# Optimization experiments

Measured on AMD Instinct MI355X. Metric: run time of the kernel, lower is better.

## Reference

```python
import jax, jax.numpy as jnp
import numpy as np

DIM = 1024
HEADS = 16
HD = DIM // HEADS          # 64
HID = 4 * DIM              # 4096
TPF = 1374                 # tokens_per_frame
LR = 0.1
NS_ITERS = 5
TTT_STEPS = 2
B, S = 2, 4
SN = S * TPF               # 5496


def _newton_schulz(G, iters=NS_ITERS):
    """Muon Newton-Schulz orthogonalization (quintic iteration)."""
    a, b, c = 3.4445, -4.7750, 2.0315
    X = G / (jnp.linalg.norm(G) + 1e-7)
    transposed = G.shape[0] > G.shape[1]
    if transposed:
        X = X.T
    for _ in range(iters):
        A = X @ X.T                      # [m,m], m = min(rows, cols)
        X = a * X + (b * A + c * (A @ A)) @ X
    return X.T if transposed else X


def _muon_update(p, g):
    return p - LR * _newton_schulz(g)


def setup_inputs() -> dict:
    key = jax.random.key(0)
    ks = jax.random.split(key, 8)
    inp = {
        "x": jax.random.normal(ks[0], (B, SN, DIM), jnp.float32),
        "qkv_w": jax.random.normal(ks[1], (DIM, 3 * DIM), jnp.float32) * (DIM ** -0.5),
        "qkv_b": jnp.zeros((3 * DIM,), jnp.float32),
        "qn_scale": jnp.ones((HD,), jnp.float32),
        "qn_bias": jnp.zeros((HD,), jnp.float32),
        "kn_scale": jnp.ones((HD,), jnp.float32),
        "kn_bias": jnp.zeros((HD,), jnp.float32),
        # theta: lecun-normal scale (std = 1/sqrt(fan_in))
        "ttt_gate": jax.random.normal(ks[2], (DIM, HID), jnp.float32) * (DIM ** -0.5),
        "ttt_val": jax.random.normal(ks[3], (DIM, HID), jnp.float32) * (DIM ** -0.5),
        "ttt_proj": jax.random.normal(ks[4], (HID, DIM), jnp.float32) * (HID ** -0.5),
        "proj_w": jax.random.normal(ks[5], (DIM, DIM), jnp.float32) * (DIM ** -0.5),
        "proj_b": jnp.zeros((DIM,), jnp.float32),
    }
    return inp


def reference(x, qkv_w, qkv_b, qn_scale, qn_bias, kn_scale, kn_bias,
              ttt_gate, ttt_val, ttt_proj, proj_w, proj_b):
    Bx, SNx, _ = x.shape
    qkv = x @ qkv_w + qkv_b                       # [B, SN, 3*DIM]
    q, k, v = jnp.split(qkv, 3, axis=-1)
    q = q.reshape(Bx, SNx, HEADS, HD)
    k = k.reshape(Bx, SNx, HEADS, HD)
    # per-head L2 normalize then affine NormLayer (x*scale + bias)
    q = q / (jnp.linalg.norm(q, axis=-1, keepdims=True) + 1e-6) * qn_scale + qn_bias
    k = k / (jnp.linalg.norm(k, axis=-1, keepdims=True) + 1e-6) * kn_scale + kn_bias
    q_ttt = q.reshape(-1, DIM)                    # [B*SN, DIM]
    k_ttt = k.reshape(-1, DIM)
    # no short_conv param at init -> v_mixed is identity, so v_target == v
    v_ttt = v.reshape(-1, DIM)

    theta = {"gate": ttt_gate, "val": ttt_val, "proj": ttt_proj}

    def loss_fn(p):
        h = jax.nn.swish(k_ttt @ p["gate"]) * (k_ttt @ p["val"])   # [B*SN, HID]
        pred = h @ p["proj"]                                        # [B*SN, DIM]
        return jnp.mean((pred - v_ttt) ** 2)

    for _ in range(TTT_STEPS):
        grads = jax.grad(loss_fn)(theta)
        theta = {kk: _muon_update(theta[kk], grads[kk]) for kk in theta}

    h_q = jax.nn.swish(q_ttt @ theta["gate"]) * (q_ttt @ theta["val"])
    o = (h_q @ theta["proj"]) @ proj_w + proj_b
    return o.reshape(Bx, SNx, DIM)
```

## Files before the change

kernel.cpp:

```cpp
#include <hip/hip_runtime.h>
#include <stdint.h>

#define NTOK 10992
#define NTOKA 11264
#define PMi 4194304

typedef unsigned short u16;
typedef __attribute__((ext_vector_type(8))) __bf16 b8;
typedef __attribute__((ext_vector_type(4))) float f32x4;

__device__ __forceinline__ u16 f2b(float f) {
  union { float f; uint32_t u; } v; v.f = f;
  return (u16)((v.u + 0x7fffu + ((v.u >> 16) & 1u)) >> 16);
}
__device__ __forceinline__ float b2f(u16 b) {
  union { uint32_t u; float f; } v; v.u = ((uint32_t)b) << 16; return v.f;
}
__device__ __forceinline__ uint2 pk4(u16 a, u16 b, u16 c, u16 d) {
  uint2 r; r.x = (uint32_t)a | ((uint32_t)b << 16); r.y = (uint32_t)c | ((uint32_t)d << 16);
  return r;
}
__device__ __forceinline__ void gload16(const u16* g, u16* l) {
  __builtin_amdgcn_global_load_lds((const __attribute__((address_space(1))) void*)(const void*)g,
                                   (__attribute__((address_space(3))) void*)(void*)l, 16, 0, 0);
}

struct GA {
  const u16* A[3]; const u16* B[3];
  void* C[3]; u16* O1[3]; u16* OT[3];
  const void* E0[3]; const u16* E1[3];
  int lda[3], ldb[3];
  int M, N, K, ldc, ldo1, ldt, lde0, lde1;
  float p0, p1;
};

template <int EPI, int SPLIT>
__global__ __launch_bounds__(256, 2) void gemm_bt(GA g) {
  __shared__ u16 As[128 * 32];
  __shared__ u16 Bs[128 * 32];
  int bz = blockIdx.z, koff = 0, klen = g.K;
  if constexpr (SPLIT) { koff = (bz & 1) * (g.K >> 1); bz >>= 1; klen = g.K >> 1; }
  const u16* __restrict__ A = g.A[bz] + koff;
  const u16* __restrict__ B = g.B[bz] + koff;
  const int lda = g.lda[bz], ldb = g.ldb[bz];
  const int m0 = blockIdx.y * 128, n0 = blockIdx.x * 128;
  const int tid = threadIdx.x, w = tid >> 6, lane = tid & 63;
  const int wr = (w >> 1) * 64, wc = (w & 1) * 64;
  const int ln = lane & 15, lq = lane >> 4;

  f32x4 acc[4][4];
#pragma unroll
  for (int i = 0; i < 4; ++i)
#pragma unroll
    for (int j = 0; j < 4; ++j)
#pragma unroll
      for (int r = 0; r < 4; ++r) acc[i][j][r] = 0.f;

  const u16* Ag = A + (size_t)(m0 + 32 * w + (lane >> 2)) * lda + (lane & 3) * 8;
  const u16* Bg = B + (size_t)(n0 + 32 * w + (lane >> 2)) * ldb + (lane & 3) * 8;
  u16* AsW = &As[w * 1024];
  u16* BsW = &Bs[w * 1024];
  const int nkt = klen >> 5;

  for (int kt = 0; kt < nkt; ++kt) {
    __syncthreads();
    gload16(Ag, AsW);
    gload16(Ag + (size_t)16 * lda, AsW + 512);
    gload16(Bg, BsW);
    gload16(Bg + (size_t)16 * ldb, BsW + 512);
    Ag += 32; Bg += 32;
    __syncthreads();
    b8 af[4], bfr[4];
#pragma unroll
    for (int i = 0; i < 4; ++i) af[i] = *(const b8*)&As[(wr + i * 16 + ln) * 32 + lq * 8];
#pragma unroll
    for (int j = 0; j < 4; ++j) bfr[j] = *(const b8*)&Bs[(wc + j * 16 + ln) * 32 + lq * 8];
#pragma unroll
    for (int i = 0; i < 4; ++i)
#pragma unroll
      for (int j = 0; j < 4; ++j)
        acc[i][j] = __builtin_amdgcn_mfma_f32_16x16x32_bf16(af[i], bfr[j], acc[i][j], 0, 0, 0);
  }

  float* Cf = (float*)g.C[bz];
  u16* Cb = (u16*)g.C[bz];
  u16* O1 = g.O1[bz];
  const float* E0f = (const float*)g.E0[bz];
  const u16* E0b = (const u16*)g.E0[bz];
  const u16* E1b = g.E1[bz];

#pragma unroll
  for (int i = 0; i < 4; ++i) {
    const int mb = m0 + wr + i * 16 + lq * 4;
    if (mb >= g.M) continue;
#pragma unroll
    for (int j = 0; j < 4; ++j) {
      const int n = n0 + wc + j * 16 + ln;
      if (n >= g.N) continue;
      float vv[4];
#pragma unroll
      for (int r = 0; r < 4; ++r) vv[r] = acc[i][j][r];
      if constexpr (EPI == 0) {
#pragma unroll
        for (int r = 0; r < 4; ++r) Cb[(size_t)(mb + r) * g.ldc + n] = f2b(vv[r]);
      } else if constexpr (EPI == 1) {
        const float bias = E0f[n];
#pragma unroll
        for (int r = 0; r < 4; ++r) Cb[(size_t)(mb + r) * g.ldc + n] = f2b(vv[r] + bias);
      } else if constexpr (EPI == 5) {
        u16 cq[4], oq[4];
#pragma unroll
        for (int r = 0; r < 4; ++r) {
          const int m = mb + r;
          const float zg = b2f(E0b[(size_t)m * g.lde0 + n]);
          const float zv = b2f(E1b[(size_t)m * g.lde1 + n]);
          const float s = 1.f / (1.f + __expf(-zg));
          cq[r] = f2b(vv[r] * zv * s * (1.f + zg * (1.f - s)));
          oq[r] = f2b(vv[r] * zg * s);
        }
        *(uint2*)&Cb[(size_t)n * g.ldt + mb] = pk4(cq[0], cq[1], cq[2], cq[3]);
        *(uint2*)&O1[(size_t)n * g.ldt + mb] = pk4(oq[0], oq[1], oq[2], oq[3]);
      } else if constexpr (EPI == 6) {
        const float bias = E0f[n];
#pragma unroll
        for (int r = 0; r < 4; ++r) Cf[(size_t)(mb + r) * g.ldc + n] = vv[r] + bias;
      } else if constexpr (EPI == 8) {
#pragma unroll
        for (int r = 0; r < 4; ++r) atomicAdd(&Cf[(size_t)(mb + r) * g.ldc + n], vv[r]);
      } else if constexpr (EPI == 16) {
        uint2 old = *(const uint2*)&Cb[(size_t)n * 1024 + mb];
        u16 nq[4];
        nq[0] = f2b(b2f((u16)(old.x & 0xffff)) - 0.1f * vv[0]);
        nq[1] = f2b(b2f((u16)(old.x >> 16)) - 0.1f * vv[1]);
        nq[2] = f2b(b2f((u16)(old.y & 0xffff)) - 0.1f * vv[2]);
        nq[3] = f2b(b2f((u16)(old.y >> 16)) - 0.1f * vv[3]);
        *(uint2*)&Cb[(size_t)n * 1024 + mb] = pk4(nq[0], nq[1], nq[2], nq[3]);
        if (O1) {
#pragma unroll
          for (int r = 0; r < 4; ++r) O1[(size_t)(mb + r) * 4096 + n] = nq[r];
        }
      }
    }
  }
}

template <int EPI>
__global__ __launch_bounds__(256, 2) void gemm_gv(GA g) {
  __shared__ u16 As[128 * 32];
  __shared__ u16 Gs[128 * 32];
  __shared__ u16 Vs[128 * 32];
  const u16* __restrict__ A = g.A[0];
  const u16* __restrict__ G = g.B[0];
  const u16* __restrict__ V = g.B[1];
  const int lda = g.lda[0], ldb = g.ldb[0];
  const int m0 = blockIdx.y * 128, n0 = blockIdx.x * 128;
  const int tid = threadIdx.x, w = tid >> 6, lane = tid & 63;
  const int wr = (w >> 1) * 64, wc = (w & 1) * 64;
  const int ln = lane & 15, lq = lane >> 4;

  f32x4 ag[4][4], av[4][4];
#pragma unroll
  for (int i = 0; i < 4; ++i)
#pragma unroll
    for (int j = 0; j < 4; ++j)
#pragma unroll
      for (int r = 0; r < 4; ++r) { ag[i][j][r] = 0.f; av[i][j][r] = 0.f; }

  const u16* Agp = A + (size_t)(m0 + 32 * w + (lane >> 2)) * lda + (lane & 3) * 8;
  const u16* Ggp = G + (size_t)(n0 + 32 * w + (lane >> 2)) * ldb + (lane & 3) * 8;
  const u16* Vgp = V + (size_t)(n0 + 32 * w + (lane >> 2)) * ldb + (lane & 3) * 8;
  u16* AsW = &As[w * 1024];
  u16* GsW = &Gs[w * 1024];
  u16* VsW = &Vs[w * 1024];
  const int nkt = g.K >> 5;

  for (int kt = 0; kt < nkt; ++kt) {
    __syncthreads();
    gload16(Agp, AsW);
    gload16(Agp + (size_t)16 * lda, AsW + 512);
    gload16(Ggp, GsW);
    gload16(Ggp + (size_t)16 * ldb, GsW + 512);
    gload16(Vgp, VsW);
    gload16(Vgp + (size_t)16 * ldb, VsW + 512);
    Agp += 32; Ggp += 32; Vgp += 32;
    __syncthreads();
    b8 af[4], gf[4], vf[4];
#pragma unroll
    for (int i = 0; i < 4; ++i) af[i] = *(const b8*)&As[(wr + i * 16 + ln) * 32 + lq * 8];
#pragma unroll
    for (int j = 0; j < 4; ++j) gf[j] = *(const b8*)&Gs[(wc + j * 16 + ln) * 32 + lq * 8];
#pragma unroll
    for (int j = 0; j < 4; ++j) vf[j] = *(const b8*)&Vs[(wc + j * 16 + ln) * 32 + lq * 8];
#pragma unroll
    for (int i = 0; i < 4; ++i)
#pragma unroll
      for (int j = 0; j < 4; ++j) {
        ag[i][j] = __builtin_amdgcn_mfma_f32_16x16x32_bf16(af[i], gf[j], ag[i][j], 0, 0, 0);
        av[i][j] = __builtin_amdgcn_mfma_f32_16x16x32_bf16(af[i], vf[j], av[i][j], 0, 0, 0);
      }
  }

  u16* Zg = (u16*)g.C[0];
  u16* Zv = g.O1[0];
  u16* Hh = g.O1[1];
  u16* HT = g.OT[0];

#pragma unroll
  for (int i = 0; i < 4; ++i) {
    const int mb = m0 + wr + i * 16 + lq * 4;
    if (mb >= g.M) continue;
#pragma unroll
    for (int j = 0; j < 4; ++j) {
      const int n = n0 + wc + j * 16 + ln;
      if (n >= g.N) continue;
      u16 hq[4];
#pragma unroll
      for (int r = 0; r < 4; ++r) {
        const int m = mb + r;
        const float zg = ag[i][j][r];
        const float zv = av[i][j][r];
        const float s = 1.f / (1.f + __expf(-zg));
        const u16 hb = f2b(zg * s * zv);
        if constexpr (EPI == 0) {
          Zg[(size_t)m * g.ldc + n] = f2b(zg);
          Zv[(size_t)m * g.ldc + n] = f2b(zv);
          Hh[(size_t)m * g.ldc + n] = hb;
          hq[r] = hb;
        } else {
          Zg[(size_t)m * g.ldc + n] = hb;
        }
      }
      if constexpr (EPI == 0)
        *(uint2*)&HT[(size_t)n * g.ldt + mb] = pk4(hq[0], hq[1], hq[2], hq[3]);
    }
  }
}

__global__ __launch_bounds__(256, 2) void fused_gg(GA ggr, GA ggv, int ysplit) {
  __shared__ u16 As[128 * 32];
  __shared__ u16 Bs[128 * 32];
  __shared__ u16 Vs[128 * 32];
  const int tid = threadIdx.x, w = tid >> 6, lane = tid & 63;
  const int wr = (w >> 1) * 64, wc = (w & 1) * 64;
  const int ln = lane & 15, lq = lane >> 4;

  if ((int)blockIdx.y < ysplit) {
    const u16* __restrict__ A = ggv.A[0];
    const u16* __restrict__ G = ggv.B[0];
    const u16* __restrict__ V = ggv.B[1];
    const int lda = ggv.lda[0], ldb = ggv.ldb[0];
    const int m0 = blockIdx.y * 128, n0 = blockIdx.x * 128;
    f32x4 ag[4][4], av[4][4];
#pragma unroll
    for (int i = 0; i < 4; ++i)
#pragma unroll
      for (int j = 0; j < 4; ++j)
#pragma unroll
        for (int r = 0; r < 4; ++r) { ag[i][j][r] = 0.f; av[i][j][r] = 0.f; }
    const u16* Agp = A + (size_t)(m0 + 32 * w + (lane >> 2)) * lda + (lane & 3) * 8;
    const u16* Ggp = G + (size_t)(n0 + 32 * w + (lane >> 2)) * ldb + (lane & 3) * 8;
    const u16* Vgp = V + (size_t)(n0 + 32 * w + (lane >> 2)) * ldb + (lane & 3) * 8;
    u16* AsW = &As[w * 1024];
    u16* GsW = &Bs[w * 1024];
    u16* VsW = &Vs[w * 1024];
    const int nkt = ggv.K >> 5;
    for (int kt = 0; kt < nkt; ++kt) {
      __syncthreads();
      gload16(Agp, AsW);
      gload16(Agp + (size_t)16 * lda, AsW + 512);
      gload16(Ggp, GsW);
      gload16(Ggp + (size_t)16 * ldb, GsW + 512);
      gload16(Vgp, VsW);
      gload16(Vgp + (size_t)16 * ldb, VsW + 512);
      Agp += 32; Ggp += 32; Vgp += 32;
      __syncthreads();
      b8 af[4], gf[4], vf[4];
#pragma unroll
      for (int i = 0; i < 4; ++i) af[i] = *(const b8*)&As[(wr + i * 16 + ln) * 32 + lq * 8];
#pragma unroll
      for (int j = 0; j < 4; ++j) gf[j] = *(const b8*)&Bs[(wc + j * 16 + ln) * 32 + lq * 8];
#pragma unroll
      for (int j = 0; j < 4; ++j) vf[j] = *(const b8*)&Vs[(wc + j * 16 + ln) * 32 + lq * 8];
#pragma unroll
      for (int i = 0; i < 4; ++i)
#pragma unroll
        for (int j = 0; j < 4; ++j) {
          ag[i][j] = __builtin_amdgcn_mfma_f32_16x16x32_bf16(af[i], gf[j], ag[i][j], 0, 0, 0);
          av[i][j] = __builtin_amdgcn_mfma_f32_16x16x32_bf16(af[i], vf[j], av[i][j], 0, 0, 0);
        }
    }
    u16* Zg = (u16*)ggv.C[0];
    u16* Zv = ggv.O1[0];
    u16* Hh = ggv.O1[1];
    u16* HT = ggv.OT[0];
#pragma unroll
    for (int i = 0; i < 4; ++i) {
      const int mb = m0 + wr + i * 16 + lq * 4;
      if (mb >= ggv.M) continue;
#pragma unroll
      for (int j = 0; j < 4; ++j) {
        const int n = n0 + wc + j * 16 + ln;
        if (n >= ggv.N) continue;
        u16 hq[4];
#pragma unroll
        for (int r = 0; r < 4; ++r) {
          const int m = mb + r;
          const float zg = ag[i][j][r];
          const float zv = av[i][j][r];
          const float s = 1.f / (1.f + __expf(-zg));
          const u16 hb = f2b(zg * s * zv);
          Zg[(size_t)m * ggv.ldc + n] = f2b(zg);
          Zv[(size_t)m * ggv.ldc + n] = f2b(zv);
          Hh[(size_t)m * ggv.ldc + n] = hb;
          hq[r] = hb;
        }
        *(uint2*)&HT[(size_t)n * ggv.ldt + mb] = pk4(hq[0], hq[1], hq[2], hq[3]);
      }
    }
  } else {
    const int yy = (int)blockIdx.y - ysplit;
    int bz = yy >> 3;
    const int m0 = (yy & 7) * 128, n0 = blockIdx.x * 128;
    const int koff = (bz & 1) * (ggr.K >> 1); bz >>= 1;
    const int klen = ggr.K >> 1;
    const u16* __restrict__ A = ggr.A[bz] + koff;
    const u16* __restrict__ B = ggr.B[bz] + koff;
    const int lda = ggr.lda[bz], ldb = ggr.ldb[bz];
    f32x4 acc[4][4];
#pragma unroll
    for (int i = 0; i < 4; ++i)
#pragma unroll
      for (int j = 0; j < 4; ++j)
#pragma unroll
        for (int r = 0; r < 4; ++r) acc[i][j][r] = 0.f;
    const u16* Ag = A + (size_t)(m0 + 32 * w + (lane >> 2)) * lda + (lane & 3) * 8;
    const u16* Bg = B + (size_t)(n0 + 32 * w + (lane >> 2)) * ldb + (lane & 3) * 8;
    u16* AsW = &As[w * 1024];
    u16* BsW = &Bs[w * 1024];
    const int nkt = klen >> 5;
    for (int kt = 0; kt < nkt; ++kt) {
      __syncthreads();
      gload16(Ag, AsW);
      gload16(Ag + (size_t)16 * lda, AsW + 512);
      gload16(Bg, BsW);
      gload16(Bg + (size_t)16 * ldb, BsW + 512);
      Ag += 32; Bg += 32;
      __syncthreads();
      b8 af[4], bfr[4];
#pragma unroll
      for (int i = 0; i < 4; ++i) af[i] = *(const b8*)&As[(wr + i * 16 + ln) * 32 + lq * 8];
#pragma unroll
      for (int j = 0; j < 4; ++j) bfr[j] = *(const b8*)&Bs[(wc + j * 16 + ln) * 32 + lq * 8];
#pragma unroll
      for (int i = 0; i < 4; ++i)
#pragma unroll
        for (int j = 0; j < 4; ++j)
          acc[i][j] = __builtin_amdgcn_mfma_f32_16x16x32_bf16(af[i], bfr[j], acc[i][j], 0, 0, 0);
    }
    float* Cf = (float*)ggr.C[bz];
#pragma unroll
    for (int i = 0; i < 4; ++i) {
      const int mb = m0 + wr + i * 16 + lq * 4;
      if (mb >= ggr.M) continue;
#pragma unroll
      for (int j = 0; j < 4; ++j) {
        const int n = n0 + wc + j * 16 + ln;
        if (n >= ggr.N) continue;
#pragma unroll
        for (int r = 0; r < 4; ++r) atomicAdd(&Cf[(size_t)(mb + r) * ggr.ldc + n], acc[i][j][r]);
      }
    }
  }
}

__global__ __launch_bounds__(256, 2) void fused_mt(GA gt, GA gm) {
  __shared__ u16 As[64 * 32];
  __shared__ u16 Bs[64 * 32];
  const int bz = blockIdx.z;
  const int mp = ((int)blockIdx.y >= 16) ? 1 : 0;
  const GA& g = mp ? gm : gt;
  const int m0 = ((int)blockIdx.y - (mp ? 16 : 0)) * 64, n0 = blockIdx.x * 64;
  const u16* __restrict__ A = g.A[bz];
  const u16* __restrict__ B = g.B[bz];
  const int lda = g.lda[bz], ldb = g.ldb[bz];
  const int tid = threadIdx.x, w = tid >> 6, lane = tid & 63;
  const int wr = (w >> 1) * 32, wc = (w & 1) * 32;
  const int ln = lane & 15, lq = lane >> 4;

  f32x4 acc[2][2];
#pragma unroll
  for (int i = 0; i < 2; ++i)
#pragma unroll
    for (int j = 0; j < 2; ++j)
#pragma unroll
      for (int r = 0; r < 4; ++r) acc[i][j][r] = 0.f;

  const u16* Ag = A + (size_t)(m0 + 16 * w + (lane >> 2)) * lda + (lane & 3) * 8;
  const u16* Bg = B + (size_t)(n0 + 16 * w + (lane >> 2)) * ldb + (lane & 3) * 8;
  u16* AsW = &As[w * 512];
  u16* BsW = &Bs[w * 512];
  const int nkt = g.K >> 5;

  for (int kt = 0; kt < nkt; ++kt) {
    __syncthreads();
    gload16(Ag, AsW);
    gload16(Bg, BsW);
    Ag += 32; Bg += 32;
    __syncthreads();
    b8 af[2], bfr[2];
#pragma unroll
    for (int i = 0; i < 2; ++i) af[i] = *(const b8*)&As[(wr + i * 16 + ln) * 32 + lq * 8];
#pragma unroll
    for (int j = 0; j < 2; ++j) bfr[j] = *(const b8*)&Bs[(wc + j * 16 + ln) * 32 + lq * 8];
#pragma unroll
    for (int i = 0; i < 2; ++i)
#pragma unroll
      for (int j = 0; j < 2; ++j)
        acc[i][j] = __builtin_amdgcn_mfma_f32_16x16x32_bf16(af[i], bfr[j], acc[i][j], 0, 0, 0);
  }

  u16* Cb = (u16*)g.C[bz];
  const u16* E0b = (const u16*)g.E0[bz];
#pragma unroll
  for (int i = 0; i < 2; ++i) {
    const int mb = m0 + wr + i * 16 + lq * 4;
#pragma unroll
    for (int j = 0; j < 2; ++j) {
      const int n = n0 + wc + j * 16 + ln;
      if (mp) {
#pragma unroll
        for (int r = 0; r < 4; ++r) {
          const int m = mb + r;
          Cb[(size_t)m * g.ldc + n] = f2b(g.p0 * b2f(E0b[(size_t)m * g.lde0 + n]) + acc[i][j][r]);
        }
      } else {
#pragma unroll
        for (int r = 0; r < 4; ++r) Cb[(size_t)(mb + r) * g.ldc + n] = f2b(acc[i][j][r]);
      }
    }
  }
}

template <int EPI>
__global__ __launch_bounds__(256, 2) void gemm64(GA g) {
  if constexpr (EPI == 10 || EPI == 11 || EPI == 12) {
    if (blockIdx.x > blockIdx.y) return;
  }
  __shared__ u16 As[64 * 32];
  __shared__ u16 Bs[64 * 32];
  const int bz = blockIdx.z;
  const u16* __restrict__ A = g.A[bz];
  const u16* __restrict__ B = g.B[bz];
  const int lda = g.lda[bz], ldb = g.ldb[bz];
  const int m0 = blockIdx.y * 64, n0 = blockIdx.x * 64;
  const int tid = threadIdx.x, w = tid >> 6, lane = tid & 63;
  const int wr = (w >> 1) * 32, wc = (w & 1) * 32;
  const int ln = lane & 15, lq = lane >> 4;

  f32x4 acc[2][2];
#pragma unroll
  for (int i = 0; i < 2; ++i)
#pragma unroll
    for (int j = 0; j < 2; ++j)
#pragma unroll
      for (int r = 0; r < 4; ++r) acc[i][j][r] = 0.f;

  const u16* Ag = A + (size_t)(m0 + 16 * w + (lane >> 2)) * lda + (lane & 3) * 8;
  const u16* Bg = B + (size_t)(n0 + 16 * w + (lane >> 2)) * ldb + (lane & 3) * 8;
  u16* AsW = &As[w * 512];
  u16* BsW = &Bs[w * 512];
  const int nkt = g.K >> 5;

  for (int kt = 0; kt < nkt; ++kt) {
    __syncthreads();
    gload16(Ag, AsW);
    gload16(Bg, BsW);
    Ag += 32; Bg += 32;
    __syncthreads();
    b8 af[2], bfr[2];
#pragma unroll
    for (int i = 0; i < 2; ++i) af[i] = *(const b8*)&As[(wr + i * 16 + ln) * 32 + lq * 8];
#pragma unroll
    for (int j = 0; j < 2; ++j) bfr[j] = *(const b8*)&Bs[(wc + j * 16 + ln) * 32 + lq * 8];
#pragma unroll
    for (int i = 0; i < 2; ++i)
#pragma unroll
      for (int j = 0; j < 2; ++j)
        acc[i][j] = __builtin_amdgcn_mfma_f32_16x16x32_bf16(af[i], bfr[j], acc[i][j], 0, 0, 0);
  }

  u16* Cb = (u16*)g.C[bz];
  u16* OT = g.OT[bz];
  const u16* E0b = (const u16*)g.E0[bz];
  const u16* E1b = g.E1[bz];
  const bool offdiag = (blockIdx.x != blockIdx.y);

#pragma unroll
  for (int i = 0; i < 2; ++i) {
    const int mb = m0 + wr + i * 16 + lq * 4;
    if (mb >= g.M) continue;
#pragma unroll
    for (int j = 0; j < 2; ++j) {
      const int n = n0 + wc + j * 16 + ln;
      if (n >= g.N) continue;
      float vv[4];
#pragma unroll
      for (int r = 0; r < 4; ++r) vv[r] = acc[i][j][r];
      if constexpr (EPI == 0) {
#pragma unroll
        for (int r = 0; r < 4; ++r) Cb[(size_t)(mb + r) * g.ldc + n] = f2b(vv[r]);
      } else if constexpr (EPI == 2) {
        u16 cq[4];
#pragma unroll
        for (int r = 0; r < 4; ++r) {
          const int m = mb + r;
          const u16 ub = f2b((vv[r] - b2f(E0b[(size_t)m * g.lde0 + n])) * g.p0);
          Cb[(size_t)m * g.ldc + n] = ub;
          cq[r] = ub;
        }
        *(uint2*)&OT[(size_t)n * g.ldt + mb] = pk4(cq[0], cq[1], cq[2], cq[3]);
      } else if constexpr (EPI == 10) {
        u16 cq[4];
#pragma unroll
        for (int r = 0; r < 4; ++r) {
          cq[r] = f2b(vv[r]);
          Cb[(size_t)(mb + r) * g.ldc + n] = cq[r];
        }
        if (offdiag)
          *(uint2*)&Cb[(size_t)n * g.ldc + mb] = pk4(cq[0], cq[1], cq[2], cq[3]);
      } else if constexpr (EPI == 11) {
        u16 cq[4];
#pragma unroll
        for (int r = 0; r < 4; ++r) {
          cq[r] = f2b(g.p0 * b2f(E0b[(size_t)(mb + r) * g.lde0 + n]) + g.p1 * vv[r]);
          Cb[(size_t)(mb + r) * g.ldc + n] = cq[r];
        }
        if (offdiag)
          *(uint2*)&Cb[(size_t)n * g.ldc + mb] = pk4(cq[0], cq[1], cq[2], cq[3]);
      } else if constexpr (EPI == 12) {
        const uint2 t2u = *(const uint2*)&E1b[(size_t)n * g.lde1 + mb];
        const float t2v[4] = { b2f((u16)(t2u.x & 0xffff)), b2f((u16)(t2u.x >> 16)),
                               b2f((u16)(t2u.y & 0xffff)), b2f((u16)(t2u.y >> 16)) };
        u16 cq[4];
#pragma unroll
        for (int r = 0; r < 4; ++r) {
          const int m = mb + r;
          const float t1 = b2f(E1b[(size_t)m * g.lde1 + n]);
          const float a0 = b2f(E0b[(size_t)m * g.lde0 + n]);
          cq[r] = f2b(g.p0 * a0 + g.p1 * (t1 + t2v[r]) + vv[r]);
          Cb[(size_t)m * g.ldc + n] = cq[r];
        }
        if (offdiag)
          *(uint2*)&Cb[(size_t)n * g.ldc + mb] = pk4(cq[0], cq[1], cq[2], cq[3]);
      } else if constexpr (EPI == 15) {
        const uint2 eu = *(const uint2*)&E0b[(size_t)n * g.lde0 + mb];
        const float e4[4] = { b2f((u16)(eu.x & 0xffff)), b2f((u16)(eu.x >> 16)),
                              b2f((u16)(eu.y & 0xffff)), b2f((u16)(eu.y >> 16)) };
#pragma unroll
        for (int r = 0; r < 4; ++r)
          Cb[(size_t)(mb + r) * g.ldc + n] = f2b(g.p0 * e4[r] + vv[r]);
      }
    }
  }
}

__global__ __launch_bounds__(256) void norm_qkv(const u16* __restrict__ qkvB,
    const float* __restrict__ qs, const float* __restrict__ qbi,
    const float* __restrict__ ks, const float* __restrict__ kbi,
    u16* __restrict__ qb, u16* __restrict__ kb, u16* __restrict__ vb) {
  const int tok = blockIdx.x;
  const int t = threadIdx.x;
  const int d = t * 4;
  const u16* row = qkvB + (size_t)tok * 3072;
  const uint2 qu = *(const uint2*)(row + d);
  const uint2 ku = *(const uint2*)(row + 1024 + d);
  *(uint2*)(vb + (size_t)tok * 1024 + d) = *(const uint2*)(row + 2048 + d);
  float q0 = b2f(qu.x & 0xffff), q1 = b2f(qu.x >> 16), q2 = b2f(qu.y & 0xffff), q3 = b2f(qu.y >> 16);
  float k0 = b2f(ku.x & 0xffff), k1 = b2f(ku.x >> 16), k2 = b2f(ku.y & 0xffff), k3 = b2f(ku.y >> 16);
  float sq = q0 * q0 + q1 * q1 + q2 * q2 + q3 * q3;
  float sk = k0 * k0 + k1 * k1 + k2 * k2 + k3 * k3;
  for (int off = 1; off < 16; off <<= 1) { sq += __shfl_xor(sq, off); sk += __shfl_xor(sk, off); }
  const float rq = 1.f / (sqrtf(sq) + 1e-6f);
  const float rk = 1.f / (sqrtf(sk) + 1e-6f);
  const int hd = d & 63;
  const float4 qsv = *(const float4*)(qs + hd);
  const float4 qbv = *(const float4*)(qbi + hd);
  const float4 ksv = *(const float4*)(ks + hd);
  const float4 kbv = *(const float4*)(kbi + hd);
  uint64_t pq = (uint64_t)f2b(q0 * rq * qsv.x + qbv.x)
              | ((uint64_t)f2b(q1 * rq * qsv.y + qbv.y) << 16)
              | ((uint64_t)f2b(q2 * rq * qsv.z + qbv.z) << 32)
              | ((uint64_t)f2b(q3 * rq * qsv.w + qbv.w) << 48);
  uint64_t pk = (uint64_t)f2b(k0 * rk * ksv.x + kbv.x)
              | ((uint64_t)f2b(k1 * rk * ksv.y + kbv.y) << 16)
              | ((uint64_t)f2b(k2 * rk * ksv.z + kbv.z) << 32)
              | ((uint64_t)f2b(k3 * rk * ksv.w + kbv.w) << 48);
  *(uint64_t*)(qb + (size_t)tok * 1024 + d) = pq;
  *(uint64_t*)(kb + (size_t)tok * 1024 + d) = pk;
}

__global__ __launch_bounds__(256) void tr_b16(const u16* __restrict__ in, u16* __restrict__ out,
                                              int Cin, int Rtot, int Rval,
                                              size_t inStr, size_t outStr) {
  const int b = blockIdx.z;
  in += (size_t)b * inStr; out += (size_t)b * outStr;
  __shared__ u16 t[32][33];
  const int c0 = blockIdx.x * 32, r0 = blockIdx.y * 32;
  const int tx = threadIdx.x, ty = threadIdx.y;
#pragma unroll
  for (int yy = 0; yy < 4; ++yy) {
    const int rr = ty * 4 + yy;
    const int r = r0 + rr;
    t[rr][tx] = (r < Rval) ? in[(size_t)r * Cin + c0 + tx] : (u16)0;
  }
  __syncthreads();
#pragma unroll
  for (int yy = 0; yy < 4; ++yy) {
    const int cc = ty * 4 + yy;
    out[(size_t)(c0 + cc) * Rtot + r0 + tx] = t[tx][cc];
  }
}

__global__ __launch_bounds__(256) void tr_f32b(const float* __restrict__ in, u16* __restrict__ out,
                                               int Cin, int Rtot) {
  __shared__ u16 t[32][33];
  const int c0 = blockIdx.x * 32, r0 = blockIdx.y * 32;
  const int tx = threadIdx.x, ty = threadIdx.y;
#pragma unroll
  for (int yy = 0; yy < 4; ++yy) {
    const int rr = ty * 4 + yy;
    t[rr][tx] = f2b(in[(size_t)(r0 + rr) * Cin + c0 + tx]);
  }
  __syncthreads();
#pragma unroll
  for (int yy = 0; yy < 4; ++yy) {
    const int cc = ty * 4 + yy;
    out[(size_t)(c0 + cc) * Rtot + r0 + tx] = t[tx][cc];
  }
}

__global__ void cvt_k(const float* __restrict__ in, u16* __restrict__ out, int n) {
  const int i = blockIdx.x * 256 + threadIdx.x;
  if (i < n) out[i] = f2b(in[i]);
}

__global__ void diag_k(float* __restrict__ out, int n, float val) {
  const int i = blockIdx.x * 256 + threadIdx.x;
  if (i < n) out[i] = val;
}

__global__ void addI_k(const u16* __restrict__ W, u16* __restrict__ M, float a) {
  const int i = blockIdx.x * 256 + threadIdx.x;
  const size_t o = (size_t)blockIdx.y * 1048576;
  u16 v = W[o + i];
  if ((i >> 10) == (i & 1023)) v = f2b(a + b2f(v));
  M[o + i] = v;
}

__global__ __launch_bounds__(256) void sumsq_k(const float* __restrict__ g, float* __restrict__ out) {
  const int b = blockIdx.y;
  const float* p = g + (size_t)b * PMi;
  float s = 0.f;
  for (int i = blockIdx.x * 256 + threadIdx.x; i < PMi; i += gridDim.x * 256) {
    float v = p[i]; s += v * v;
  }
  for (int off = 32; off > 0; off >>= 1) s += __shfl_xor(s, off);
  __shared__ float red[4];
  if ((threadIdx.x & 63) == 0) red[threadIdx.x >> 6] = s;
  __syncthreads();
  if (threadIdx.x == 0) atomicAdd(out + b, red[0] + red[1] + red[2] + red[3]);
}

__global__ __launch_bounds__(256) void scale_tr(const float* __restrict__ g, const float* __restrict__ ss,
                                                u16* __restrict__ Xb, u16* __restrict__ XbT) {
  const int b = blockIdx.z;
  __shared__ u16 t[32][33];
  const float r = 1.f / (sqrtf(ss[b]) + 1e-7f);
  const float* G = g + (size_t)b * PMi;
  u16* X = Xb + (size_t)b * PMi;
  u16* XT = XbT + (size_t)b * PMi;
  const int j0 = blockIdx.x * 32, i0 = blockIdx.y * 32;
  const int tx = threadIdx.x, ty = threadIdx.y;
#pragma unroll
  for (int yy = 0; yy < 4; ++yy) {
    const int rr = ty * 4 + yy;
    const u16 v = f2b(G[(size_t)(i0 + rr) * 4096 + j0 + tx] * r);
    X[(size_t)(i0 + rr) * 4096 + j0 + tx] = v;
    t[rr][tx] = v;
  }
  __syncthreads();
#pragma unroll
  for (int yy = 0; yy < 4; ++yy) {
    const int cc = ty * 4 + yy;
    XT[(size_t)(j0 + cc) * 1024 + i0 + tx] = t[tx][cc];
  }
}

static GA mk(const u16* A, const u16* B, void* C, int M, int N, int K,
             int lda, int ldb, int ldc) {
  GA a{};
  a.A[0] = a.A[1] = a.A[2] = A;
  a.B[0] = a.B[1] = a.B[2] = B;
  a.C[0] = a.C[1] = a.C[2] = C;
  a.lda[0] = a.lda[1] = a.lda[2] = lda;
  a.ldb[0] = a.ldb[1] = a.ldb[2] = ldb;
  a.M = M; a.N = N; a.K = K; a.ldc = ldc;
  return a;
}

extern "C" void kernel_launch(void* const* d_in, const int* in_sizes, int n_in,
                              void* d_out, int out_size, void* d_ws, size_t ws_size,
                              hipStream_t stream) {
  (void)in_sizes; (void)n_in;
  const float* x      = (const float*)d_in[0];
  const float* qkv_w  = (const float*)d_in[1];
  const float* qkv_b  = (const float*)d_in[2];
  const float* qn_s   = (const float*)d_in[3];
  const float* qn_b   = (const float*)d_in[4];
  const float* kn_s   = (const float*)d_in[5];
  const float* kn_b   = (const float*)d_in[6];
  const float* g_gate = (const float*)d_in[7];
  const float* g_val  = (const float*)d_in[8];
  const float* g_proj = (const float*)d_in[9];
  const float* proj_w = (const float*)d_in[10];
  const float* proj_b = (const float*)d_in[11];
  float* out = (float*)d_out;

  const size_t PM = PMi;
  const size_t TD = (size_t)NTOKA * 1024;
  const size_t PERS = 127926528ull;

  auto needP = [&](int chk) {
    return PERS + 7ull * (size_t)chk * 8192 + 2ull * (size_t)chk * 2048 + 50331648ull + 8192;
  };
  auto needU = [&](int chk) {
    return PERS + 5ull * (size_t)chk * 8192 + 2ull * (size_t)chk * 2048 + 50331648ull + 4096;
  };
  int CHKr, PAIRED;
  if      (ws_size >= needP(5632)) { CHKr = 5632; PAIRED = 1; }
  else if (ws_size >= needU(5632)) { CHKr = 5632; PAIRED = 0; }
  else if (ws_size >= needP(2816)) { CHKr = 2816; PAIRED = 1; }
  else if (ws_size >= needP(2560)) { CHKr = 2560; PAIRED = 1; }
  else if (ws_size >= needP(2304)) { CHKr = 2304; PAIRED = 1; }
  else if (ws_size >= needP(2048)) { CHKr = 2048; PAIRED = 1; }
  else if (ws_size >= needU(1408)) { CHKr = 1408; PAIRED = 0; }
  else {
    diag_k<<<dim3((out_size + 255) / 256), dim3(256), 0, stream>>>(out, out_size,
                                                                   (float)(ws_size >> 20));
    return;
  }

  char* p = (char*)d_ws;
  auto carve = [&](size_t bytes) { char* r = p; p += (bytes + 255) & ~(size_t)255; return (void*)r; };
  auto cdiv = [](int a, int b) { return (a + b - 1) / b; };

  u16* Gt     = (u16*)carve(PM * 2);
  u16* Vt     = (u16*)carve(PM * 2);
  u16* Pt     = (u16*)carve(PM * 2);
  u16* Pb     = (u16*)carve(PM * 2);
  u16* projWt = (u16*)carve(1048576ull * 2);
  u16* qb     = (u16*)carve(TD * 2);
  u16* kb     = (u16*)carve(TD * 2);
  u16* vT     = (u16*)carve(TD * 2);
  u16* kT     = (u16*)carve(TD * 2);
  float* ssq  = (float*)carve(256);
  char* arena = p;

  u16* xb     = (u16*)arena;
  u16* qkvWt  = (u16*)(arena + 23068672);
  u16* qkvB   = (u16*)(arena + 29360128);
  u16* vb_tmp = (u16*)(arena + 96894976);
  const size_t CB = (size_t)CHKr * 4096 * 2;
  const size_t DP = (size_t)CHKr * 1024 * 2;
  u16* zg     = (u16*)arena;
  u16* zv     = (u16*)(arena + CB);
  u16* hh0    = (u16*)(arena + 2 * CB);
  u16* hT0    = (u16*)(arena + 3 * CB);
  u16* dzvT   = (u16*)(arena + 4 * CB);
  u16* dpredT = (u16*)(arena + 5 * CB);
  u16* dpredb = (u16*)(arena + 5 * CB + DP);
  float* gAll = (float*)(arena + 5 * CB + 2 * DP);
  u16* hh1    = PAIRED ? (u16*)(arena + 5 * CB + 2 * DP + 3 * PM * 4) : hh0;
  u16* hT1    = PAIRED ? (u16*)(arena + 6 * CB + 2 * DP + 3 * PM * 4) : hT0;
  u16* hhA[2] = {hh0, hh1};
  u16* hTA[2] = {hT0, hT1};
  u16* XAb  = (u16*)arena;
  u16* XAbT = (u16*)(arena + 25165824);
  u16* Ab   = (u16*)(arena + 50331648);
  u16* Wb   = (u16*)(arena + 56623104);
  u16* Tb   = (u16*)(arena + 62914560);
  u16* Mb0  = (u16*)(arena + 69206016);
  u16* Mb1  = (u16*)(arena + 75497472);
  u16* hbuf = (u16*)arena;
  u16* PWt  = (u16*)(arena + 92274688);

  const dim3 blk(256), tb32(32, 8);
  const float inv2 = 2.0f / (10992.0f * 1024.0f);
  const float nsa = 3.4445f, nsb = -4.7750f, nsc = 2.0315f;

  cvt_k<<<dim3(43968), blk, 0, stream>>>(x, xb, NTOK * 1024);
  cvt_k<<<dim3(16384), blk, 0, stream>>>(g_proj, Pb, (int)PM);
  tr_f32b<<<dim3(96, 32), tb32, 0, stream>>>(qkv_w, qkvWt, 3072, 1024);
  tr_f32b<<<dim3(32, 32), tb32, 0, stream>>>(proj_w, projWt, 1024, 1024);
  tr_f32b<<<dim3(128, 32), tb32, 0, stream>>>(g_gate, Gt, 4096, 1024);
  tr_f32b<<<dim3(128, 32), tb32, 0, stream>>>(g_val, Vt, 4096, 1024);
  tr_f32b<<<dim3(32, 128), tb32, 0, stream>>>(g_proj, Pt, 1024, 4096);

  {
    GA a = mk(xb, qkvWt, qkvB, NTOK, 3072, 1024, 1024, 1024, 3072);
    a.E0[0] = a.E0[1] = a.E0[2] = qkv_b;
    gemm_bt<1, 0><<<dim3(24, 86, 1), blk, 0, stream>>>(a);
  }
  norm_qkv<<<dim3(NTOK), blk, 0, stream>>>(qkvB, qn_s, qn_b, kn_s, kn_b, qb, kb, vb_tmp);
  tr_b16<<<dim3(32, 352, 1), tb32, 0, stream>>>(kb, kT, 1024, NTOKA, NTOK, 0, 0);
  tr_b16<<<dim3(32, 352, 1), tb32, 0, stream>>>(vb_tmp, vT, 1024, NTOKA, NTOK, 0, 0);

  for (int step = 0; step < 2; ++step) {
    hipMemsetAsync(gAll, 0, 3 * PM * 4, stream);
    int havePend = 0;
    GA pendGA{};
    for (int ci = 0, c0 = 0; c0 < NTOK; ++ci, c0 += CHKr) {
      const int vc = (NTOK - c0 < CHKr) ? (NTOK - c0) : CHKr;
      const int mt = cdiv(vc, 128);
      const u16* kc = kb + (size_t)c0 * 1024;
      u16* hhp = hhA[ci & 1];
      u16* hTp = hTA[ci & 1];
      if (vc < CHKr)
        hipMemsetAsync(hTp, 0, CB, stream);
      {
        GA agv{};
        agv.A[0] = kc; agv.lda[0] = 1024;
        agv.B[0] = Gt; agv.B[1] = Vt; agv.ldb[0] = 1024;
        agv.C[0] = zg; agv.O1[0] = zv; agv.O1[1] = hhp; agv.OT[0] = hTp;
        agv.M = vc; agv.N = 4096; agv.K = 1024; agv.ldc = 4096; agv.ldt = CHKr;
        if (PAIRED && havePend) {
          fused_gg<<<dim3(32, mt + 48, 1), blk, 0, stream>>>(pendGA, agv, mt);
          havePend = 0;
        } else {
          gemm_gv<0><<<dim3(32, mt, 1), blk, 0, stream>>>(agv);
        }
      }
      if (vc < CHKr) {
        hipMemsetAsync(dzvT, 0, CB, stream);
        hipMemsetAsync(dpredT, 0, DP, stream);
      }
      {
        GA a = mk(Pt, hhp, dpredT, 1024, vc, 4096, 4096, 4096, CHKr);
        a.OT[0] = dpredb; a.ldt = 1024;
        a.E0[0] = vT + c0; a.lde0 = NTOKA; a.p0 = inv2;
        gemm64<2><<<dim3(cdiv(vc, 64), 16, 1), blk, 0, stream>>>(a);
      }
      if (vc < CHKr)
        hipMemsetAsync(hhp, 0, CB, stream);
      {
        GA a = mk(dpredb, Pb, hhp, vc, 4096, 1024, 1024, 1024, 0);
        a.O1[0] = dzvT; a.ldt = CHKr;
        a.E0[0] = zg; a.lde0 = 4096; a.E1[0] = zv; a.lde1 = 4096;
        gemm_bt<5, 0><<<dim3(32, mt, 1), blk, 0, stream>>>(a);
      }
      {
        GA a{};
        a.A[0] = kT + c0; a.A[1] = kT + c0; a.A[2] = dpredT;
        a.lda[0] = NTOKA; a.lda[1] = NTOKA; a.lda[2] = CHKr;
        a.B[0] = hhp; a.B[1] = dzvT; a.B[2] = hTp;
        a.ldb[0] = a.ldb[1] = a.ldb[2] = CHKr;
        a.C[0] = gAll; a.C[1] = gAll + PM; a.C[2] = gAll + 2 * PM;
        a.M = 1024; a.N = 4096; a.K = CHKr; a.ldc = 4096;
        const int last = (c0 + CHKr >= NTOK);
        if (PAIRED && !last) { pendGA = a; havePend = 1; }
        else gemm_bt<8, 1><<<dim3(32, 8, 6), blk, 0, stream>>>(a);
      }
    }
    hipMemsetAsync(ssq, 0, 16, stream);
    sumsq_k<<<dim3(512, 3), blk, 0, stream>>>(gAll, ssq);
    scale_tr<<<dim3(128, 32, 3), tb32, 0, stream>>>(gAll, ssq, XAb, XAbT);

    {
      GA a{};
      for (int b = 0; b < 3; ++b) {
        a.A[b] = XAb + (size_t)b * PM; a.B[b] = XAb + (size_t)b * PM;
        a.C[b] = Ab + (size_t)b * 1048576;
        a.lda[b] = 4096; a.ldb[b] = 4096;
      }
      a.M = 1024; a.N = 1024; a.K = 4096; a.ldc = 1024;
      gemm64<10><<<dim3(16, 16, 3), blk, 0, stream>>>(a);
    }
    for (int it = 0; it < 5; ++it) {
      {
        GA a{};
        for (int b = 0; b < 3; ++b) {
          a.A[b] = Ab + (size_t)b * 1048576; a.B[b] = Ab + (size_t)b * 1048576;
          a.C[b] = Wb + (size_t)b * 1048576; a.E0[b] = Ab + (size_t)b * 1048576;
          a.lda[b] = 1024; a.ldb[b] = 1024;
        }
        a.M = 1024; a.N = 1024; a.K = 1024; a.ldc = 1024; a.lde0 = 1024;
        a.p0 = nsb; a.p1 = nsc;
        gemm64<11><<<dim3(16, 16, 3), blk, 0, stream>>>(a);
      }
      if (it == 0) {
        addI_k<<<dim3(4096, 3), blk, 0, stream>>>(Wb, Mb0, nsa);
        {
          GA a{};
          for (int b = 0; b < 3; ++b) {
            a.A[b] = Wb + (size_t)b * 1048576; a.B[b] = Ab + (size_t)b * 1048576;
            a.C[b] = Tb + (size_t)b * 1048576;
            a.lda[b] = 1024; a.ldb[b] = 1024;
          }
          a.M = 1024; a.N = 1024; a.K = 1024; a.ldc = 1024;
          gemm64<0><<<dim3(16, 16, 3), blk, 0, stream>>>(a);
        }
      } else if (it < 4) {
        u16* Mti = (it & 1) ? Mb0 : Mb1;
        u16* Mto = (it & 1) ? Mb1 : Mb0;
        GA gt{}, gm{};
        for (int b = 0; b < 3; ++b) {
          gt.A[b] = Wb + (size_t)b * 1048576; gt.B[b] = Ab + (size_t)b * 1048576;
          gt.C[b] = Tb + (size_t)b * 1048576;
          gt.lda[b] = 1024; gt.ldb[b] = 1024;
          gm.A[b] = Mti + (size_t)b * 1048576; gm.B[b] = Wb + (size_t)b * 1048576;
          gm.C[b] = Mto + (size_t)b * 1048576; gm.E0[b] = Mti + (size_t)b * 1048576;
          gm.lda[b] = 1024; gm.ldb[b] = 1024;
        }
        gt.M = gt.N = 1024; gt.K = 1024; gt.ldc = 1024;
        gm.M = gm.N = 1024; gm.K = 1024; gm.ldc = 1024; gm.lde0 = 1024; gm.p0 = nsa;
        fused_mt<<<dim3(16, 32, 3), blk, 0, stream>>>(gt, gm);
      } else {
        GA a{};
        for (int b = 0; b < 3; ++b) {
          a.A[b] = Wb + (size_t)b * 1048576; a.B[b] = Mb1 + (size_t)b * 1048576;
          a.C[b] = Mb0 + (size_t)b * 1048576; a.E0[b] = Mb1 + (size_t)b * 1048576;
          a.lda[b] = 1024; a.ldb[b] = 1024;
        }
        a.M = 1024; a.N = 1024; a.K = 1024; a.ldc = 1024; a.lde0 = 1024; a.p0 = nsa;
        gemm64<15><<<dim3(16, 16, 3), blk, 0, stream>>>(a);
      }
      if (it < 4) {
        GA a{};
        for (int b = 0; b < 3; ++b) {
          a.A[b] = Tb + (size_t)b * 1048576; a.B[b] = Wb + (size_t)b * 1048576;
          a.C[b] = Ab + (size_t)b * 1048576;
          a.E0[b] = Ab + (size_t)b * 1048576; a.E1[b] = Tb + (size_t)b * 1048576;
          a.lda[b] = 1024; a.ldb[b] = 1024;
        }
        a.M = 1024; a.N = 1024; a.K = 1024; a.ldc = 1024;
        a.lde0 = 1024; a.lde1 = 1024;
        a.p0 = nsa * nsa; a.p1 = nsa;
        gemm64<12><<<dim3(16, 16, 3), blk, 0, stream>>>(a);
      }
    }
    {
      GA a{};
      for (int b = 0; b < 3; ++b) {
        a.A[b] = Mb0 + (size_t)b * 1048576; a.B[b] = XAbT + (size_t)b * PM;
        a.lda[b] = 1024; a.ldb[b] = 1024;
      }
      a.C[0] = Gt; a.C[1] = Vt; a.C[2] = Pb;
      a.O1[0] = nullptr; a.O1[1] = nullptr; a.O1[2] = Pt;
      a.M = 1024; a.N = 4096; a.K = 1024; a.ldc = 1024;
      gemm_bt<16, 0><<<dim3(32, 8, 3), blk, 0, stream>>>(a);
    }
  }

  gemm_bt<0, 0><<<dim3(32, 8, 1), blk, 0, stream>>>(
      mk(projWt, Pb, PWt, 1024, 4096, 1024, 1024, 1024, 4096));
  {
    GA a{};
    a.A[0] = qb; a.lda[0] = 1024;
    a.B[0] = Gt; a.B[1] = Vt; a.ldb[0] = 1024;
    a.C[0] = hbuf;
    a.M = NTOK; a.N = 4096; a.K = 1024; a.ldc = 4096;
    gemm_gv<1><<<dim3(32, 86, 1), blk, 0, stream>>>(a);
  }
  {
    GA a = mk(hbuf, PWt, out, NTOK, 1024, 4096, 4096, 4096, 1024);
    a.E0[0] = proj_b;
    gemm_bt<6, 0><<<dim3(8, 86, 1), blk, 0, stream>>>(a);
  }
}
```

Measured before the change: 5.622 ms.

## Fuse QKV normalization, pipeline TTT chunks across kernels, precompute swish-derivative factors

Adds a QKV GEMM kernel with bias, per-head L2 normalization and affine scaling in its epilogue, writing q, k, kT and vT directly. The gate/value epilogue now stores precomputed swish-derivative factors, so the backward epilogue only multiplies. A new MODE 2 schedule software-pipelines the chunk loop with double-buffered intermediates: it co-launches each chunk's forward GEMM with the previous chunk's dh GEMM, and its grad-accumulation GEMM with the current chunk's dpred GEMM. The final projection-weight GEMM is also merged with the q gate/value GEMM. This cuts launch count and fills idle CUs, at the cost of more buffers and more complex kernels.

After: 5.569 ms. About the same (-0.9%).

```diff
diff --git a/kernel.cpp b/kernel.cpp
--- a/kernel.cpp
+++ b/kernel.cpp
@@ -112,11 +112,10 @@
 #pragma unroll
         for (int r = 0; r < 4; ++r) {
           const int m = mb + r;
-          const float zg = b2f(E0b[(size_t)m * g.lde0 + n]);
-          const float zv = b2f(E1b[(size_t)m * g.lde1 + n]);
-          const float s = 1.f / (1.f + __expf(-zg));
-          cq[r] = f2b(vv[r] * zv * s * (1.f + zg * (1.f - s)));
-          oq[r] = f2b(vv[r] * zg * s);
+          const float f1 = b2f(E0b[(size_t)m * g.lde0 + n]);
+          const float f2 = b2f(E1b[(size_t)m * g.lde1 + n]);
+          cq[r] = f2b(vv[r] * f1);
+          oq[r] = f2b(vv[r] * f2);
         }
         *(uint2*)&Cb[(size_t)n * g.ldt + mb] = pk4(cq[0], cq[1], cq[2], cq[3]);
         *(uint2*)&O1[(size_t)n * g.ldt + mb] = pk4(oq[0], oq[1], oq[2], oq[3]);
@@ -138,6 +137,123 @@
         if (O1) {
 #pragma unroll
           for (int r = 0; r < 4; ++r) O1[(size_t)(mb + r) * 4096 + n] = nq[r];
+        }
+      }
+    }
+  }
+}
+
+__global__ __launch_bounds__(256, 2) void gemm_qkv(GA g) {
+  __shared__ u16 As[128 * 32];
+  __shared__ u16 Bs[128 * 32];
+  const u16* __restrict__ A = g.A[0];
+  const u16* __restrict__ B = g.B[0];
+  const int lda = g.lda[0], ldb = g.ldb[0];
+  const int m0 = blockIdx.y * 128, n0 = blockIdx.x * 128;
+  const int tid = threadIdx.x, w = tid >> 6, lane = tid & 63;
+  const int wr = (w >> 1) * 64, wc = (w & 1) * 64;
+  const int ln = lane & 15, lq = lane >> 4;
+
+  f32x4 acc[4][4];
+#pragma unroll
+  for (int i = 0; i < 4; ++i)
+#pragma unroll
+    for (int j = 0; j < 4; ++j)
+#pragma unroll
+      for (int r = 0; r < 4; ++r) acc[i][j][r] = 0.f;
+
+  const u16* Ag = A + (size_t)(m0 + 32 * w + (lane >> 2)) * lda + (lane & 3) * 8;
+  const u16* Bg = B + (size_t)(n0 + 32 * w + (lane >> 2)) * ldb + (lane & 3) * 8;
+  u16* AsW = &As[w * 1024];
+  u16* BsW = &Bs[w * 1024];
+  const int nkt = g.K >> 5;
+
+  for (int kt = 0; kt < nkt; ++kt) {
+    __syncthreads();
+    gload16(Ag, AsW);
+    gload16(Ag + (size_t)16 * lda, AsW + 512);
+    gload16(Bg, BsW);
+    gload16(Bg + (size_t)16 * ldb, BsW + 512);
+    Ag += 32; Bg += 32;
+    __syncthreads();
+    b8 af[4], bfr[4];
+#pragma unroll
+    for (int i = 0; i < 4; ++i) af[i] = *(const b8*)&As[(wr + i * 16 + ln) * 32 + lq * 8];
+#pragma unroll
+    for (int j = 0; j < 4; ++j) bfr[j] = *(const b8*)&Bs[(wc + j * 16 + ln) * 32 + lq * 8];
+#pragma unroll
+    for (int i = 0; i < 4; ++i)
+#pragma unroll
+      for (int j = 0; j < 4; ++j)
+        acc[i][j] = __builtin_amdgcn_mfma_f32_16x16x32_bf16(af[i], bfr[j], acc[i][j], 0, 0, 0);
+  }
+
+  u16* qbp = (u16*)g.C[0];
+  u16* kbp = g.O1[0];
+  u16* kTp = g.OT[0];
+  u16* vTp = g.OT[1];
+  const float* bias = (const float*)g.E0[0];
+  const float* qS = (const float*)g.E0[1];
+  const float* kS = (const float*)g.E0[2];
+  const float* qB = (const float*)g.E1[0];
+  const float* kB = (const float*)g.E1[1];
+  const int seg = (n0 + wc) >> 10;
+
+#pragma unroll
+  for (int i = 0; i < 4; ++i) {
+    const int mb = m0 + wr + i * 16 + lq * 4;
+    if (mb >= g.M) continue;
+    float vb4[4][4];
+    float s4[4] = {0.f, 0.f, 0.f, 0.f};
+#pragma unroll
+    for (int j = 0; j < 4; ++j) {
+      const int n = n0 + wc + j * 16 + ln;
+      const float bs = bias[n];
+#pragma unroll
+      for (int r = 0; r < 4; ++r) {
+        const float v = acc[i][j][r] + bs;
+        vb4[j][r] = v;
+        s4[r] += v * v;
+      }
+    }
+    if (seg == 2) {
+#pragma unroll
+      for (int j = 0; j < 4; ++j) {
+        const int n = n0 + wc + j * 16 + ln;
+        *(uint2*)&vTp[(size_t)(n - 2048) * NTOKA + mb] =
+            pk4(f2b(vb4[j][0]), f2b(vb4[j][1]), f2b(vb4[j][2]), f2b(vb4[j][3]));
+      }
+    } else {
+#pragma unroll
+      for (int off = 1; off < 16; off <<= 1)
+#pragma unroll
+        for (int r = 0; r < 4; ++r) s4[r] += __shfl_xor(s4[r], off);
+      float rinv[4];
+#pragma unroll
+      for (int r = 0; r < 4; ++r) rinv[r] = 1.f / (sqrtf(s4[r]) + 1e-6f);
+      if (seg == 0) {
+#pragma unroll
+        for (int j = 0; j < 4; ++j) {
+          const int n = n0 + wc + j * 16 + ln;
+          const int hd = n & 63;
+          const float sc = qS[hd], bi = qB[hd];
+#pragma unroll
+          for (int r = 0; r < 4; ++r)
+            qbp[(size_t)(mb + r) * 1024 + n] = f2b(vb4[j][r] * rinv[r] * sc + bi);
+        }
+      } else {
+#pragma unroll
+        for (int j = 0; j < 4; ++j) {
+          const int n = n0 + wc + j * 16 + ln;
+          const int hd = n & 63;
+          const float sc = kS[hd], bi = kB[hd];
+          u16 kq[4];
+#pragma unroll
+          for (int r = 0; r < 4; ++r) {
+            kq[r] = f2b(vb4[j][r] * rinv[r] * sc + bi);
+            kbp[(size_t)(mb + r) * 1024 + (n - 1024)] = kq[r];
+          }
+          *(uint2*)&kTp[(size_t)(n - 1024) * NTOKA + mb] = pk4(kq[0], kq[1], kq[2], kq[3]);
         }
       }
     }
@@ -200,8 +316,8 @@
       }
   }
 
-  u16* Zg = (u16*)g.C[0];
-  u16* Zv = g.O1[0];
+  u16* F1 = (u16*)g.C[0];
+  u16* F2 = g.O1[0];
   u16* Hh = g.O1[1];
   u16* HT = g.OT[0];
 
@@ -220,14 +336,15 @@
         const float zg = ag[i][j][r];
         const float zv = av[i][j][r];
         const float s = 1.f / (1.f + __expf(-zg));
-        const u16 hb = f2b(zg * s * zv);
+        const float sw = zg * s;
         if constexpr (EPI == 0) {
-          Zg[(size_t)m * g.ldc + n] = f2b(zg);
-          Zv[(size_t)m * g.ldc + n] = f2b(zv);
+          F1[(size_t)m * g.ldc + n] = f2b(zv * s * (1.f + zg * (1.f - s)));
+          F2[(size_t)m * g.ldc + n] = f2b(sw);
+          const u16 hb = f2b(sw * zv);
           Hh[(size_t)m * g.ldc + n] = hb;
           hq[r] = hb;
         } else {
-          Zg[(size_t)m * g.ldc + n] = hb;
+          F1[(size_t)m * g.ldc + n] = f2b(sw * zv);
         }
       }
       if constexpr (EPI == 0)
@@ -289,8 +406,8 @@
           av[i][j] = __builtin_amdgcn_mfma_f32_16x16x32_bf16(af[i], vf[j], av[i][j], 0, 0, 0);
         }
     }
-    u16* Zg = (u16*)ggv.C[0];
-    u16* Zv = ggv.O1[0];
+    u16* F1 = (u16*)ggv.C[0];
+    u16* F2 = ggv.O1[0];
     u16* Hh = ggv.O1[1];
     u16* HT = ggv.OT[0];
 #pragma unroll
@@ -308,9 +425,10 @@
           const float zg = ag[i][j][r];
           const float zv = av[i][j][r];
           const float s = 1.f / (1.f + __expf(-zg));
-          const u16 hb = f2b(zg * s * zv);
-          Zg[(size_t)m * ggv.ldc + n] = f2b(zg);
-          Zv[(size_t)m * ggv.ldc + n] = f2b(zv);
+          const float sw = zg * s;
+          F1[(size_t)m * ggv.ldc + n] = f2b(zv * s * (1.f + zg * (1.f - s)));
+          F2[(size_t)m * ggv.ldc + n] = f2b(sw);
+          const u16 hb = f2b(sw * zv);
           Hh[(size_t)m * ggv.ldc + n] = hb;
           hq[r] = hb;
         }
@@ -373,6 +491,271 @@
   }
 }
 
+__global__ __launch_bounds__(256, 2) void fused_hg(GA gdh, GA ggv, int ysplit) {
+  __shared__ u16 As[128 * 32];
+  __shared__ u16 Bs[128 * 32];
+  __shared__ u16 Vs[128 * 32];
+  const int tid = threadIdx.x, w = tid >> 6, lane = tid & 63;
+  const int wr = (w >> 1) * 64, wc = (w & 1) * 64;
+  const int ln = lane & 15, lq = lane >> 4;
+
+  if ((int)blockIdx.y < ysplit) {
+    const u16* __restrict__ A = ggv.A[0];
+    const u16* __restrict__ G = ggv.B[0];
+    const u16* __restrict__ V = ggv.B[1];
+    const int lda = ggv.lda[0], ldb = ggv.ldb[0];
+    const int m0 = blockIdx.y * 128, n0 = blockIdx.x * 128;
+    f32x4 ag[4][4], av[4][4];
+#pragma unroll
+    for (int i = 0; i < 4; ++i)
+#pragma unroll
+      for (int j = 0; j < 4; ++j)
+#pragma unroll
+        for (int r = 0; r < 4; ++r) { ag[i][j][r] = 0.f; av[i][j][r] = 0.f; }
+    const u16* Agp = A + (size_t)(m0 + 32 * w + (lane >> 2)) * lda + (lane & 3) * 8;
+    const u16* Ggp = G + (size_t)(n0 + 32 * w + (lane >> 2)) * ldb + (lane & 3) * 8;
+    const u16* Vgp = V + (size_t)(n0 + 32 * w + (lane >> 2)) * ldb + (lane & 3) * 8;
+    u16* AsW = &As[w * 1024];
+    u16* GsW = &Bs[w * 1024];
+    u16* VsW = &Vs[w * 1024];
+    const int nkt = ggv.K >> 5;
+    for (int kt = 0; kt < nkt; ++kt) {
+      __syncthreads();
+      gload16(Agp, AsW);
+      gload16(Agp + (size_t)16 * lda, AsW + 512);
+      gload16(Ggp, GsW);
+      gload16(Ggp + (size_t)16 * ldb, GsW + 512);
+      gload16(Vgp, VsW);
+      gload16(Vgp + (size_t)16 * ldb, VsW + 512);
+      Agp += 32; Ggp += 32; Vgp += 32;
+      __syncthreads();
+      b8 af[4], gf[4], vf[4];
+#pragma unroll
+      for (int i = 0; i < 4; ++i) af[i] = *(const b8*)&As[(wr + i * 16 + ln) * 32 + lq * 8];
+#pragma unroll
+      for (int j = 0; j < 4; ++j) gf[j] = *(const b8*)&Bs[(wc + j * 16 + ln) * 32 + lq * 8];
+#pragma unroll
+      for (int j = 0; j < 4; ++j) vf[j] = *(const b8*)&Vs[(wc + j * 16 + ln) * 32 + lq * 8];
+#pragma unroll
+      for (int i = 0; i < 4; ++i)
+#pragma unroll
+        for (int j = 0; j < 4; ++j) {
+          ag[i][j] = __builtin_amdgcn_mfma_f32_16x16x32_bf16(af[i], gf[j], ag[i][j], 0, 0, 0);
+          av[i][j] = __builtin_amdgcn_mfma_f32_16x16x32_bf16(af[i], vf[j], av[i][j], 0, 0, 0);
+        }
+    }
+    u16* F1 = (u16*)ggv.C[0];
+    u16* F2 = ggv.O1[0];
+    u16* Hh = ggv.O1[1];
+    u16* HT = ggv.OT[0];
+#pragma unroll
+    for (int i = 0; i < 4; ++i) {
+      const int mb = m0 + wr + i * 16 + lq * 4;
+      if (mb >= ggv.M) continue;
+#pragma unroll
+      for (int j = 0; j < 4; ++j) {
+        const int n = n0 + wc + j * 16 + ln;
+        u16 hq[4];
+#pragma unroll
+        for (int r = 0; r < 4; ++r) {
+          const int m = mb + r;
+          const float zg = ag[i][j][r];
+          const float zv = av[i][j][r];
+          const float s = 1.f / (1.f + __expf(-zg));
+          const float sw = zg * s;
+          F1[(size_t)m * ggv.ldc + n] = f2b(zv * s * (1.f + zg * (1.f - s)));
+          F2[(size_t)m * ggv.ldc + n] = f2b(sw);
+          const u16 hb = f2b(sw * zv);
+          Hh[(size_t)m * ggv.ldc + n] = hb;
+          hq[r] = hb;
+        }
+        *(uint2*)&HT[(size_t)n * ggv.ldt + mb] = pk4(hq[0], hq[1], hq[2], hq[3]);
+      }
+    }
+  } else {
+    const int m0 = ((int)blockIdx.y - ysplit) * 128, n0 = blockIdx.x * 128;
+    const u16* __restrict__ A = gdh.A[0];
+    const u16* __restrict__ B = gdh.B[0];
+    const int lda = gdh.lda[0], ldb = gdh.ldb[0];
+    f32x4 acc[4][4];
+#pragma unroll
+    for (int i = 0; i < 4; ++i)
+#pragma unroll
+      for (int j = 0; j < 4; ++j)
+#pragma unroll
+        for (int r = 0; r < 4; ++r) acc[i][j][r] = 0.f;
+    const u16* Ag = A + (size_t)(m0 + 32 * w + (lane >> 2)) * lda + (lane & 3) * 8;
+    const u16* Bg = B + (size_t)(n0 + 32 * w + (lane >> 2)) * ldb + (lane & 3) * 8;
+    u16* AsW = &As[w * 1024];
+    u16* BsW = &Bs[w * 1024];
+    const int nkt = gdh.K >> 5;
+    for (int kt = 0; kt < nkt; ++kt) {
+      __syncthreads();
+      gload16(Ag, AsW);
+      gload16(Ag + (size_t)16 * lda, AsW + 512);
+      gload16(Bg, BsW);
+      gload16(Bg + (size_t)16 * ldb, BsW + 512);
+      Ag += 32; Bg += 32;
+      __syncthreads();
+      b8 af[4], bfr[4];
+#pragma unroll
+      for (int i = 0; i < 4; ++i) af[i] = *(const b8*)&As[(wr + i * 16 + ln) * 32 + lq * 8];
+#pragma unroll
+      for (int j = 0; j < 4; ++j) bfr[j] = *(const b8*)&Bs[(wc + j * 16 + ln) * 32 + lq * 8];
+#pragma unroll
+      for (int i = 0; i < 4; ++i)
+#pragma unroll
+        for (int j = 0; j < 4; ++j)
+          acc[i][j] = __builtin_amdgcn_mfma_f32_16x16x32_bf16(af[i], bfr[j], acc[i][j], 0, 0, 0);
+    }
+    u16* Cb = (u16*)gdh.C[0];
+    u16* O1 = gdh.O1[0];
+    const u16* E0b = (const u16*)gdh.E0[0];
+    const u16* E1b = gdh.E1[0];
+#pragma unroll
+    for (int i = 0; i < 4; ++i) {
+      const int mb = m0 + wr + i * 16 + lq * 4;
+      if (mb >= gdh.M) continue;
+#pragma unroll
+      for (int j = 0; j < 4; ++j) {
+        const int n = n0 + wc + j * 16 + ln;
+        u16 cq[4], oq[4];
+#pragma unroll
+        for (int r = 0; r < 4; ++r) {
+          const int m = mb + r;
+          const float f1 = b2f(E0b[(size_t)m * gdh.lde0 + n]);
+          const float f2 = b2f(E1b[(size_t)m * gdh.lde1 + n]);
+          cq[r] = f2b(acc[i][j][r] * f1);
+          oq[r] = f2b(acc[i][j][r] * f2);
+        }
+        *(uint2*)&Cb[(size_t)n * gdh.ldt + mb] = pk4(cq[0], cq[1], cq[2], cq[3]);
+        *(uint2*)&O1[(size_t)n * gdh.ldt + mb] = pk4(oq[0], oq[1], oq[2], oq[3]);
+      }
+    }
+  }
+}
+
+__global__ __launch_bounds__(256, 2) void fused_gd(GA ggr, GA gdp, int nGr, int dpx) {
+  __shared__ u16 As[128 * 32];
+  __shared__ u16 Bs[128 * 32];
+  const int tid = threadIdx.x, w = tid >> 6, lane = tid & 63;
+  const int ln = lane & 15, lq = lane >> 4;
+  const int bid = blockIdx.x;
+
+  if (bid < nGr) {
+    const int wr = (w >> 1) * 64, wc = (w & 1) * 64;
+    const int n0 = (bid & 31) * 128;
+    const int rest = bid >> 5;
+    const int m0 = (rest & 7) * 128;
+    int bz = rest >> 3;
+    const int koff = (bz & 1) * (ggr.K >> 1); bz >>= 1;
+    const int klen = ggr.K >> 1;
+    const u16* __restrict__ A = ggr.A[bz] + koff;
+    const u16* __restrict__ B = ggr.B[bz] + koff;
+    const int lda = ggr.lda[bz], ldb = ggr.ldb[bz];
+    f32x4 acc[4][4];
+#pragma unroll
+    for (int i = 0; i < 4; ++i)
+#pragma unroll
+      for (int j = 0; j < 4; ++j)
+#pragma unroll
+        for (int r = 0; r < 4; ++r) acc[i][j][r] = 0.f;
+    const u16* Ag = A + (size_t)(m0 + 32 * w + (lane >> 2)) * lda + (lane & 3) * 8;
+    const u16* Bg = B + (size_t)(n0 + 32 * w + (lane >> 2)) * ldb + (lane & 3) * 8;
+    u16* AsW = &As[w * 1024];
+    u16* BsW = &Bs[w * 1024];
+    const int nkt = klen >> 5;
+    for (int kt = 0; kt < nkt; ++kt) {
+      __syncthreads();
+      gload16(Ag, AsW);
+      gload16(Ag + (size_t)16 * lda, AsW + 512);
+      gload16(Bg, BsW);
+      gload16(Bg + (size_t)16 * ldb, BsW + 512);
+      Ag += 32; Bg += 32;
+      __syncthreads();
+      b8 af[4], bfr[4];
+#pragma unroll
+      for (int i = 0; i < 4; ++i) af[i] = *(const b8*)&As[(wr + i * 16 + ln) * 32 + lq * 8];
+#pragma unroll
+      for (int j = 0; j < 4; ++j) bfr[j] = *(const b8*)&Bs[(wc + j * 16 + ln) * 32 + lq * 8];
+#pragma unroll
+      for (int i = 0; i < 4; ++i)
+#pragma unroll
+        for (int j = 0; j < 4; ++j)
+          acc[i][j] = __builtin_amdgcn_mfma_f32_16x16x32_bf16(af[i], bfr[j], acc[i][j], 0, 0, 0);
+    }
+    float* Cf = (float*)ggr.C[bz];
+#pragma unroll
+    for (int i = 0; i < 4; ++i) {
+      const int mb = m0 + wr + i * 16 + lq * 4;
+#pragma unroll
+      for (int j = 0; j < 4; ++j) {
+        const int n = n0 + wc + j * 16 + ln;
+#pragma unroll
+        for (int r = 0; r < 4; ++r) atomicAdd(&Cf[(size_t)(mb + r) * ggr.ldc + n], acc[i][j][r]);
+      }
+    }
+  } else {
+    const int wr = (w >> 1) * 32, wc = (w & 1) * 32;
+    const int l = bid - nGr;
+    const int n0 = (l % dpx) * 64;
+    const int m0 = (l / dpx) * 64;
+    const u16* __restrict__ A = gdp.A[0];
+    const u16* __restrict__ B = gdp.B[0];
+    const int lda = gdp.lda[0], ldb = gdp.ldb[0];
+    f32x4 acc[2][2];
+#pragma unroll
+    for (int i = 0; i < 2; ++i)
+#pragma unroll
+      for (int j = 0; j < 2; ++j)
+#pragma unroll
+        for (int r = 0; r < 4; ++r) acc[i][j][r] = 0.f;
+    const u16* Ag = A + (size_t)(m0 + 16 * w + (lane >> 2)) * lda + (lane & 3) * 8;
+    const u16* Bg = B + (size_t)(n0 + 16 * w + (lane >> 2)) * ldb + (lane & 3) * 8;
+    u16* AsW = &As[w * 512];
+    u16* BsW = &Bs[w * 512];
+    const int nkt = gdp.K >> 5;
+    for (int kt = 0; kt < nkt; ++kt) {
+      __syncthreads();
+      gload16(Ag, AsW);
+      gload16(Bg, BsW);
+      Ag += 32; Bg += 32;
+      __syncthreads();
+      b8 af[2], bfr[2];
+#pragma unroll
+      for (int i = 0; i < 2; ++i) af[i] = *(const b8*)&As[(wr + i * 16 + ln) * 32 + lq * 8];
+#pragma unroll
+      for (int j = 0; j < 2; ++j) bfr[j] = *(const b8*)&Bs[(wc + j * 16 + ln) * 32 + lq * 8];
+#pragma unroll
+      for (int i = 0; i < 2; ++i)
+#pragma unroll
+        for (int j = 0; j < 2; ++j)
+          acc[i][j] = __builtin_amdgcn_mfma_f32_16x16x32_bf16(af[i], bfr[j], acc[i][j], 0, 0, 0);
+    }
+    u16* Cb = (u16*)gdp.C[0];
+    u16* OT = gdp.OT[0];
+    const u16* E0b = (const u16*)gdp.E0[0];
+#pragma unroll
+    for (int i = 0; i < 2; ++i) {
+      const int mb = m0 + wr + i * 16 + lq * 4;
+#pragma unroll
+      for (int j = 0; j < 2; ++j) {
+        const int n = n0 + wc + j * 16 + ln;
+        if (n >= gdp.N) continue;
+        u16 cq[4];
+#pragma unroll
+        for (int r = 0; r < 4; ++r) {
+          const int m = mb + r;
+          const u16 ub = f2b((acc[i][j][r] - b2f(E0b[(size_t)m * gdp.lde0 + n])) * gdp.p0);
+          Cb[(size_t)m * gdp.ldc + n] = ub;
+          cq[r] = ub;
+        }
+        *(uint2*)&OT[(size_t)n * gdp.ldt + mb] = pk4(cq[0], cq[1], cq[2], cq[3]);
+      }
+    }
+  }
+}
+
 __global__ __launch_bounds__(256, 2) void fused_mt(GA gt, GA gm) {
   __shared__ u16 As[64 * 32];
   __shared__ u16 Bs[64 * 32];
@@ -441,6 +824,126 @@
   }
 }
 
+__global__ __launch_bounds__(256, 2) void fused_pg(GA gp, GA ggv, int ysplit) {
+  __shared__ u16 As[128 * 32];
+  __shared__ u16 Bs[128 * 32];
+  __shared__ u16 Vs[128 * 32];
+  const int tid = threadIdx.x, w = tid >> 6, lane = tid & 63;
+  const int wr = (w >> 1) * 64, wc = (w & 1) * 64;
+  const int ln = lane & 15, lq = lane >> 4;
+
+  if ((int)blockIdx.y < ysplit) {
+    const u16* __restrict__ A = ggv.A[0];
+    const u16* __restrict__ G = ggv.B[0];
+    const u16* __restrict__ V = ggv.B[1];
+    const int lda = ggv.lda[0], ldb = ggv.ldb[0];
+    const int m0 = blockIdx.y * 128, n0 = blockIdx.x * 128;
+    f32x4 ag[4][4], av[4][4];
+#pragma unroll
+    for (int i = 0; i < 4; ++i)
+#pragma unroll
+      for (int j = 0; j < 4; ++j)
+#pragma unroll
+        for (int r = 0; r < 4; ++r) { ag[i][j][r] = 0.f; av[i][j][r] = 0.f; }
+    const u16* Agp = A + (size_t)(m0 + 32 * w + (lane >> 2)) * lda + (lane & 3) * 8;
+    const u16* Ggp = G + (size_t)(n0 + 32 * w + (lane >> 2)) * ldb + (lane & 3) * 8;
+    const u16* Vgp = V + (size_t)(n0 + 32 * w + (lane >> 2)) * ldb + (lane & 3) * 8;
+    u16* AsW = &As[w * 1024];
+    u16* GsW = &Bs[w * 1024];
+    u16* VsW = &Vs[w * 1024];
+    const int nkt = ggv.K >> 5;
+    for (int kt = 0; kt < nkt; ++kt) {
+      __syncthreads();
+      gload16(Agp, AsW);
+      gload16(Agp + (size_t)16 * lda, AsW + 512);
+      gload16(Ggp, GsW);
+      gload16(Ggp + (size_t)16 * ldb, GsW + 512);
+      gload16(Vgp, VsW);
+      gload16(Vgp + (size_t)16 * ldb, VsW + 512);
+      Agp += 32; Ggp += 32; Vgp += 32;
+      __syncthreads();
+      b8 af[4], gf[4], vf[4];
+#pragma unroll
+      for (int i = 0; i < 4; ++i) af[i] = *(const b8*)&As[(wr + i * 16 + ln) * 32 + lq * 8];
+#pragma unroll
+      for (int j = 0; j < 4; ++j) gf[j] = *(const b8*)&Bs[(wc + j * 16 + ln) * 32 + lq * 8];
+#pragma unroll
+      for (int j = 0; j < 4; ++j) vf[j] = *(const b8*)&Vs[(wc + j * 16 + ln) * 32 + lq * 8];
+#pragma unroll
+      for (int i = 0; i < 4; ++i)
+#pragma unroll
+        for (int j = 0; j < 4; ++j) {
+          ag[i][j] = __builtin_amdgcn_mfma_f32_16x16x32_bf16(af[i], gf[j], ag[i][j], 0, 0, 0);
+          av[i][j] = __builtin_amdgcn_mfma_f32_16x16x32_bf16(af[i], vf[j], av[i][j], 0, 0, 0);
+        }
+    }
+    u16* Hh = (u16*)ggv.C[0];
+#pragma unroll
+    for (int i = 0; i < 4; ++i) {
+      const int mb = m0 + wr + i * 16 + lq * 4;
+      if (mb >= ggv.M) continue;
+#pragma unroll
+      for (int j = 0; j < 4; ++j) {
+        const int n = n0 + wc + j * 16 + ln;
+#pragma unroll
+        for (int r = 0; r < 4; ++r) {
+          const float zg = ag[i][j][r];
+          const float zv = av[i][j][r];
+          const float s = 1.f / (1.f + __expf(-zg));
+          Hh[(size_t)(mb + r) * ggv.ldc + n] = f2b(zg * s * zv);
+        }
+      }
+    }
+  } else {
+    const int m0 = ((int)blockIdx.y - ysplit) * 128, n0 = blockIdx.x * 128;
+    const u16* __restrict__ A = gp.A[0];
+    const u16* __restrict__ B = gp.B[0];
+    const int lda = gp.lda[0], ldb = gp.ldb[0];
+    f32x4 acc[4][4];
+#pragma unroll
+    for (int i = 0; i < 4; ++i)
+#pragma unroll
+      for (int j = 0; j < 4; ++j)
+#pragma unroll
+        for (int r = 0; r < 4; ++r) acc[i][j][r] = 0.f;
+    const u16* Ag = A + (size_t)(m0 + 32 * w + (lane >> 2)) * lda + (lane & 3) * 8;
+    const u16* Bg = B + (size_t)(n0 + 32 * w + (lane >> 2)) * ldb + (lane & 3) * 8;
+    u16* AsW = &As[w * 1024];
+    u16* BsW = &Bs[w * 1024];
+    const int nkt = gp.K >> 5;
+    for (int kt = 0; kt < nkt; ++kt) {
+      __syncthreads();
+      gload16(Ag, AsW);
+      gload16(Ag + (size_t)16 * lda, AsW + 512);
+      gload16(Bg, BsW);
+      gload16(Bg + (size_t)16 * ldb, BsW + 512);
+      Ag += 32; Bg += 32;
+      __syncthreads();
+      b8 af[4], bfr[4];
+#pragma unroll
+      for (int i = 0; i < 4; ++i) af[i] = *(const b8*)&As[(wr + i * 16 + ln) * 32 + lq * 8];
+#pragma unroll
+      for (int j = 0; j < 4; ++j) bfr[j] = *(const b8*)&Bs[(wc + j * 16 + ln) * 32 + lq * 8];
+#pragma unroll
+      for (int i = 0; i < 4; ++i)
+#pragma unroll
+        for (int j = 0; j < 4; ++j)
+          acc[i][j] = __builtin_amdgcn_mfma_f32_16x16x32_bf16(af[i], bfr[j], acc[i][j], 0, 0, 0);
+    }
+    u16* Cb = (u16*)gp.C[0];
+#pragma unroll
+    for (int i = 0; i < 4; ++i) {
+      const int mb = m0 + wr + i * 16 + lq * 4;
+#pragma unroll
+      for (int j = 0; j < 4; ++j) {
+        const int n = n0 + wc + j * 16 + ln;
+#pragma unroll
+        for (int r = 0; r < 4; ++r) Cb[(size_t)(mb + r) * gp.ldc + n] = f2b(acc[i][j][r]);
+      }
+    }
+  }
+}
+
 template <int EPI>
 __global__ __launch_bounds__(256, 2) void gemm64(GA g) {
   if constexpr (EPI == 10 || EPI == 11 || EPI == 12) {
@@ -561,63 +1064,6 @@
           Cb[(size_t)(mb + r) * g.ldc + n] = f2b(g.p0 * e4[r] + vv[r]);
       }
     }
-  }
-}
-
-__global__ __launch_bounds__(256) void norm_qkv(const u16* __restrict__ qkvB,
-    const float* __restrict__ qs, const float* __restrict__ qbi,
-    const float* __restrict__ ks, const float* __restrict__ kbi,
-    u16* __restrict__ qb, u16* __restrict__ kb, u16* __restrict__ vb) {
-  const int tok = blockIdx.x;
-  const int t = threadIdx.x;
-  const int d = t * 4;
-  const u16* row = qkvB + (size_t)tok * 3072;
-  const uint2 qu = *(const uint2*)(row + d);
-  const uint2 ku = *(const uint2*)(row + 1024 + d);
-  *(uint2*)(vb + (size_t)tok * 1024 + d) = *(const uint2*)(row + 2048 + d);
-  float q0 = b2f(qu.x & 0xffff), q1 = b2f(qu.x >> 16), q2 = b2f(qu.y & 0xffff), q3 = b2f(qu.y >> 16);
-  float k0 = b2f(ku.x & 0xffff), k1 = b2f(ku.x >> 16), k2 = b2f(ku.y & 0xffff), k3 = b2f(ku.y >> 16);
-  float sq = q0 * q0 + q1 * q1 + q2 * q2 + q3 * q3;
-  float sk = k0 * k0 + k1 * k1 + k2 * k2 + k3 * k3;
-  for (int off = 1; off < 16; off <<= 1) { sq += __shfl_xor(sq, off); sk += __shfl_xor(sk, off); }
-  const float rq = 1.f / (sqrtf(sq) + 1e-6f);
-  const float rk = 1.f / (sqrtf(sk) + 1e-6f);
-  const int hd = d & 63;
-  const float4 qsv = *(const float4*)(qs + hd);
-  const float4 qbv = *(const float4*)(qbi + hd);
-  const float4 ksv = *(const float4*)(ks + hd);
-  const float4 kbv = *(const float4*)(kbi + hd);
-  uint64_t pq = (uint64_t)f2b(q0 * rq * qsv.x + qbv.x)
-              | ((uint64_t)f2b(q1 * rq * qsv.y + qbv.y) << 16)
-              | ((uint64_t)f2b(q2 * rq * qsv.z + qbv.z) << 32)
-              | ((uint64_t)f2b(q3 * rq * qsv.w + qbv.w) << 48);
-  uint64_t pk = (uint64_t)f2b(k0 * rk * ksv.x + kbv.x)
-              | ((uint64_t)f2b(k1 * rk * ksv.y + kbv.y) << 16)
-              | ((uint64_t)f2b(k2 * rk * ksv.z + kbv.z) << 32)
-              | ((uint64_t)f2b(k3 * rk * ksv.w + kbv.w) << 48);
-  *(uint64_t*)(qb + (size_t)tok * 1024 + d) = pq;
-  *(uint64_t*)(kb + (size_t)tok * 1024 + d) = pk;
-}
-
-__global__ __launch_bounds__(256) void tr_b16(const u16* __restrict__ in, u16* __restrict__ out,
-                                              int Cin, int Rtot, int Rval,
-                                              size_t inStr, size_t outStr) {
-  const int b = blockIdx.z;
-  in += (size_t)b * inStr; out += (size_t)b * outStr;
-  __shared__ u16 t[32][33];
-  const int c0 = blockIdx.x * 32, r0 = blockIdx.y * 32;
-  const int tx = threadIdx.x, ty = threadIdx.y;
-#pragma unroll
-  for (int yy = 0; yy < 4; ++yy) {
-    const int rr = ty * 4 + yy;
-    const int r = r0 + rr;
-    t[rr][tx] = (r < Rval) ? in[(size_t)r * Cin + c0 + tx] : (u16)0;
-  }
-  __syncthreads();
-#pragma unroll
-  for (int yy = 0; yy < 4; ++yy) {
-    const int cc = ty * 4 + yy;
-    out[(size_t)(c0 + cc) * Rtot + r0 + tx] = t[tx][cc];
   }
 }
 
@@ -730,20 +1176,23 @@
   const size_t TD = (size_t)NTOKA * 1024;
   const size_t PERS = 127926528ull;
 
+  auto needD = [&](int chk) {
+    return PERS + 9ull * (size_t)chk * 8192 + 4ull * (size_t)chk * 2048 + 50331648ull + 8192;
+  };
   auto needP = [&](int chk) {
     return PERS + 7ull * (size_t)chk * 8192 + 2ull * (size_t)chk * 2048 + 50331648ull + 8192;
   };
   auto needU = [&](int chk) {
     return PERS + 5ull * (size_t)chk * 8192 + 2ull * (size_t)chk * 2048 + 50331648ull + 4096;
   };
-  int CHKr, PAIRED;
-  if      (ws_size >= needP(5632)) { CHKr = 5632; PAIRED = 1; }
-  else if (ws_size >= needU(5632)) { CHKr = 5632; PAIRED = 0; }
-  else if (ws_size >= needP(2816)) { CHKr = 2816; PAIRED = 1; }
-  else if (ws_size >= needP(2560)) { CHKr = 2560; PAIRED = 1; }
-  else if (ws_size >= needP(2304)) { CHKr = 2304; PAIRED = 1; }
-  else if (ws_size >= needP(2048)) { CHKr = 2048; PAIRED = 1; }
-  else if (ws_size >= needU(1408)) { CHKr = 1408; PAIRED = 0; }
+  int CHKr, MODE;
+  if      (ws_size >= needD(5632)) { CHKr = 5632; MODE = 2; }
+  else if (ws_size >= needD(4096)) { CHKr = 4096; MODE = 2; }
+  else if (ws_size >= needP(5632)) { CHKr = 5632; MODE = 1; }
+  else if (ws_size >= needU(5632)) { CHKr = 5632; MODE = 0; }
+  else if (ws_size >= needP(2816)) { CHKr = 2816; MODE = 1; }
+  else if (ws_size >= needP(2048)) { CHKr = 2048; MODE = 1; }
+  else if (ws_size >= needU(1408)) { CHKr = 1408; MODE = 0; }
   else {
     diag_k<<<dim3((out_size + 255) / 256), dim3(256), 0, stream>>>(out, out_size,
                                                                    (float)(ws_size >> 20));
@@ -766,24 +1215,33 @@
   float* ssq  = (float*)carve(256);
   char* arena = p;
 
-  u16* xb     = (u16*)arena;
-  u16* qkvWt  = (u16*)(arena + 23068672);
-  u16* qkvB   = (u16*)(arena + 29360128);
-  u16* vb_tmp = (u16*)(arena + 96894976);
+  u16* xb    = (u16*)arena;
+  u16* qkvWt = (u16*)(arena + 23068672);
   const size_t CB = (size_t)CHKr * 4096 * 2;
   const size_t DP = (size_t)CHKr * 1024 * 2;
-  u16* zg     = (u16*)arena;
-  u16* zv     = (u16*)(arena + CB);
-  u16* hh0    = (u16*)(arena + 2 * CB);
-  u16* hT0    = (u16*)(arena + 3 * CB);
-  u16* dzvT   = (u16*)(arena + 4 * CB);
-  u16* dpredT = (u16*)(arena + 5 * CB);
-  u16* dpredb = (u16*)(arena + 5 * CB + DP);
-  float* gAll = (float*)(arena + 5 * CB + 2 * DP);
-  u16* hh1    = PAIRED ? (u16*)(arena + 5 * CB + 2 * DP + 3 * PM * 4) : hh0;
-  u16* hT1    = PAIRED ? (u16*)(arena + 6 * CB + 2 * DP + 3 * PM * 4) : hT0;
-  u16* hhA[2] = {hh0, hh1};
-  u16* hTA[2] = {hT0, hT1};
+  u16 *f1A[2], *f2A[2], *hhA[2], *hTA[2], *dpTA[2], *dpBA[2], *dzvT;
+  float* gAll;
+  if (MODE == 2) {
+    f1A[0] = (u16*)(arena + 0 * CB);  f2A[0] = (u16*)(arena + 1 * CB);
+    hhA[0] = (u16*)(arena + 2 * CB);  hTA[0] = (u16*)(arena + 3 * CB);
+    f1A[1] = (u16*)(arena + 4 * CB);  f2A[1] = (u16*)(arena + 5 * CB);
+    hhA[1] = (u16*)(arena + 6 * CB);  hTA[1] = (u16*)(arena + 7 * CB);
+    dzvT   = (u16*)(arena + 8 * CB);
+    dpTA[0] = (u16*)(arena + 9 * CB);          dpBA[0] = (u16*)(arena + 9 * CB + DP);
+    dpTA[1] = (u16*)(arena + 9 * CB + 2 * DP); dpBA[1] = (u16*)(arena + 9 * CB + 3 * DP);
+    gAll = (float*)(arena + 9 * CB + 4 * DP);
+  } else {
+    f1A[0] = f1A[1] = (u16*)arena;
+    f2A[0] = f2A[1] = (u16*)(arena + CB);
+    hhA[0] = (u16*)(arena + 2 * CB);
+    hTA[0] = (u16*)(arena + 3 * CB);
+    dzvT   = (u16*)(arena + 4 * CB);
+    dpTA[0] = dpTA[1] = (u16*)(arena + 5 * CB);
+    dpBA[0] = dpBA[1] = (u16*)(arena + 5 * CB + DP);
+    gAll = (float*)(arena + 5 * CB + 2 * DP);
+    hhA[1] = (MODE == 1) ? (u16*)(arena + 5 * CB + 2 * DP + 3 * PM * 4) : hhA[0];
+    hTA[1] = (MODE == 1) ? (u16*)(arena + 6 * CB + 2 * DP + 3 * PM * 4) : hTA[0];
+  }
   u16* XAb  = (u16*)arena;
   u16* XAbT = (u16*)(arena + 25165824);
   u16* Ab   = (u16*)(arena + 50331648);
@@ -798,6 +1256,8 @@
   const float inv2 = 2.0f / (10992.0f * 1024.0f);
   const float nsa = 3.4445f, nsb = -4.7750f, nsc = 2.0315f;
 
+  hipMemsetAsync(kT, 0, TD * 2, stream);
+  hipMemsetAsync(vT, 0, TD * 2, stream);
   cvt_k<<<dim3(43968), blk, 0, stream>>>(x, xb, NTOK * 1024);
   cvt_k<<<dim3(16384), blk, 0, stream>>>(g_proj, Pb, (int)PM);
   tr_f32b<<<dim3(96, 32), tb32, 0, stream>>>(qkv_w, qkvWt, 3072, 1024);
@@ -807,68 +1267,133 @@
   tr_f32b<<<dim3(32, 128), tb32, 0, stream>>>(g_proj, Pt, 1024, 4096);
 
   {
-    GA a = mk(xb, qkvWt, qkvB, NTOK, 3072, 1024, 1024, 1024, 3072);
-    a.E0[0] = a.E0[1] = a.E0[2] = qkv_b;
-    gemm_bt<1, 0><<<dim3(24, 86, 1), blk, 0, stream>>>(a);
-  }
-  norm_qkv<<<dim3(NTOK), blk, 0, stream>>>(qkvB, qn_s, qn_b, kn_s, kn_b, qb, kb, vb_tmp);
-  tr_b16<<<dim3(32, 352, 1), tb32, 0, stream>>>(kb, kT, 1024, NTOKA, NTOK, 0, 0);
-  tr_b16<<<dim3(32, 352, 1), tb32, 0, stream>>>(vb_tmp, vT, 1024, NTOKA, NTOK, 0, 0);
+    GA a = mk(xb, qkvWt, qb, NTOK, 3072, 1024, 1024, 1024, 1024);
+    a.O1[0] = kb; a.OT[0] = kT; a.OT[1] = vT;
+    a.E0[0] = qkv_b; a.E0[1] = qn_s; a.E0[2] = kn_s;
+    a.E1[0] = (const u16*)qn_b; a.E1[1] = (const u16*)kn_b;
+    gemm_qkv<<<dim3(24, 86, 1), blk, 0, stream>>>(a);
+  }
 
   for (int step = 0; step < 2; ++step) {
     hipMemsetAsync(gAll, 0, 3 * PM * 4, stream);
-    int havePend = 0;
-    GA pendGA{};
-    for (int ci = 0, c0 = 0; c0 < NTOK; ++ci, c0 += CHKr) {
-      const int vc = (NTOK - c0 < CHKr) ? (NTOK - c0) : CHKr;
-      const int mt = cdiv(vc, 128);
-      const u16* kc = kb + (size_t)c0 * 1024;
-      u16* hhp = hhA[ci & 1];
-      u16* hTp = hTA[ci & 1];
-      if (vc < CHKr)
-        hipMemsetAsync(hTp, 0, CB, stream);
+    if (MODE == 2) {
+      const int NC = cdiv(NTOK, CHKr);
+      int c0P = 0, vcP = 0, mtP = 0;
+      for (int ci = 0; ci < NC; ++ci) {
+        const int c0 = ci * CHKr;
+        const int vc = (NTOK - c0 < CHKr) ? (NTOK - c0) : CHKr;
+        const int mt = cdiv(vc, 128);
+        const int par = ci & 1, parP = par ^ 1;
+        const int tail = (ci == NC - 1 && vc < CHKr);
+        if (tail) hipMemsetAsync(hTA[par], 0, CB, stream);
+        GA agv{};
+        agv.A[0] = kb + (size_t)c0 * 1024; agv.lda[0] = 1024;
+        agv.B[0] = Gt; agv.B[1] = Vt; agv.ldb[0] = 1024;
+        agv.C[0] = f1A[par]; agv.O1[0] = f2A[par]; agv.O1[1] = hhA[par]; agv.OT[0] = hTA[par];
+        agv.M = vc; agv.N = 4096; agv.K = 1024; agv.ldc = 4096; agv.ldt = CHKr;
+        if (ci == 0) {
+          gemm_gv<0><<<dim3(32, mt, 1), blk, 0, stream>>>(agv);
+        } else {
+          GA adh{};
+          adh.A[0] = dpBA[parP]; adh.B[0] = Pb; adh.lda[0] = 1024; adh.ldb[0] = 1024;
+          adh.C[0] = hhA[parP]; adh.O1[0] = dzvT;
+          adh.E0[0] = f1A[parP]; adh.E1[0] = f2A[parP];
+          adh.M = vcP; adh.N = 4096; adh.K = 1024; adh.ldt = CHKr;
+          adh.lde0 = 4096; adh.lde1 = 4096;
+          fused_hg<<<dim3(32, mt + mtP, 1), blk, 0, stream>>>(adh, agv, mt);
+        }
+        if (tail) hipMemsetAsync(dpTA[par], 0, DP, stream);
+        GA adp = mk(Pt, hhA[par], dpTA[par], 1024, vc, 4096, 4096, 4096, CHKr);
+        adp.OT[0] = dpBA[par]; adp.ldt = 1024;
+        adp.E0[0] = vT + c0; adp.lde0 = NTOKA; adp.p0 = inv2;
+        const int dpx = cdiv(vc, 64);
+        if (ci == 0) {
+          gemm64<2><<<dim3(dpx, 16, 1), blk, 0, stream>>>(adp);
+        } else {
+          GA agr{};
+          agr.A[0] = kT + c0P; agr.A[1] = kT + c0P; agr.A[2] = dpTA[parP];
+          agr.lda[0] = NTOKA; agr.lda[1] = NTOKA; agr.lda[2] = CHKr;
+          agr.B[0] = hhA[parP]; agr.B[1] = dzvT; agr.B[2] = hTA[parP];
+          agr.ldb[0] = agr.ldb[1] = agr.ldb[2] = CHKr;
+          agr.C[0] = gAll; agr.C[1] = gAll + PM; agr.C[2] = gAll + 2 * PM;
+          agr.M = 1024; agr.N = 4096; agr.K = CHKr; agr.ldc = 4096;
+          fused_gd<<<dim3(1536 + dpx * 16, 1, 1), blk, 0, stream>>>(agr, adp, 1536, dpx);
+        }
+        c0P = c0; vcP = vc; mtP = mt;
+      }
+      const int par = (NC - 1) & 1;
+      if (vcP < CHKr) {
+        hipMemsetAsync(hhA[par], 0, CB, stream);
+        hipMemsetAsync(dzvT, 0, CB, stream);
+      }
       {
-        GA agv{};
-        agv.A[0] = kc; agv.lda[0] = 1024;
-        agv.B[0] = Gt; agv.B[1] = Vt; agv.ldb[0] = 1024;
-        agv.C[0] = zg; agv.O1[0] = zv; agv.O1[1] = hhp; agv.OT[0] = hTp;
-        agv.M = vc; agv.N = 4096; agv.K = 1024; agv.ldc = 4096; agv.ldt = CHKr;
-        if (PAIRED && havePend) {
-          fused_gg<<<dim3(32, mt + 48, 1), blk, 0, stream>>>(pendGA, agv, mt);
-          havePend = 0;
-        } else {
-          gemm_gv<0><<<dim3(32, mt, 1), blk, 0, stream>>>(agv);
-        }
-      }
-      if (vc < CHKr) {
-        hipMemsetAsync(dzvT, 0, CB, stream);
-        hipMemsetAsync(dpredT, 0, DP, stream);
+        GA adh = mk(dpBA[par], Pb, hhA[par], vcP, 4096, 1024, 1024, 1024, 0);
+        adh.O1[0] = dzvT; adh.ldt = CHKr;
+        adh.E0[0] = f1A[par]; adh.lde0 = 4096; adh.E1[0] = f2A[par]; adh.lde1 = 4096;
+        gemm_bt<5, 0><<<dim3(32, mtP, 1), blk, 0, stream>>>(adh);
       }
       {
-        GA a = mk(Pt, hhp, dpredT, 1024, vc, 4096, 4096, 4096, CHKr);
-        a.OT[0] = dpredb; a.ldt = 1024;
-        a.E0[0] = vT + c0; a.lde0 = NTOKA; a.p0 = inv2;
-        gemm64<2><<<dim3(cdiv(vc, 64), 16, 1), blk, 0, stream>>>(a);
-      }
-      if (vc < CHKr)
-        hipMemsetAsync(hhp, 0, CB, stream);
-      {
-        GA a = mk(dpredb, Pb, hhp, vc, 4096, 1024, 1024, 1024, 0);
-        a.O1[0] = dzvT; a.ldt = CHKr;
-        a.E0[0] = zg; a.lde0 = 4096; a.E1[0] = zv; a.lde1 = 4096;
-        gemm_bt<5, 0><<<dim3(32, mt, 1), blk, 0, stream>>>(a);
-      }
-      {
-        GA a{};
-        a.A[0] = kT + c0; a.A[1] = kT + c0; a.A[2] = dpredT;
-        a.lda[0] = NTOKA; a.lda[1] = NTOKA; a.lda[2] = CHKr;
-        a.B[0] = hhp; a.B[1] = dzvT; a.B[2] = hTp;
-        a.ldb[0] = a.ldb[1] = a.ldb[2] = CHKr;
-        a.C[0] = gAll; a.C[1] = gAll + PM; a.C[2] = gAll + 2 * PM;
-        a.M = 1024; a.N = 4096; a.K = CHKr; a.ldc = 4096;
-        const int last = (c0 + CHKr >= NTOK);
-        if (PAIRED && !last) { pendGA = a; havePend = 1; }
-        else gemm_bt<8, 1><<<dim3(32, 8, 6), blk, 0, stream>>>(a);
+        GA agr{};
+        agr.A[0] = kT + c0P; agr.A[1] = kT + c0P; agr.A[2] = dpTA[par];
+        agr.lda[0] = NTOKA; agr.lda[1] = NTOKA; agr.lda[2] = CHKr;
+        agr.B[0] = hhA[par]; agr.B[1] = dzvT; agr.B[2] = hTA[par];
+        agr.ldb[0] = agr.ldb[1] = agr.ldb[2] = CHKr;
+        agr.C[0] = gAll; agr.C[1] = gAll + PM; agr.C[2] = gAll + 2 * PM;
+        agr.M = 1024; agr.N = 4096; agr.K = CHKr; agr.ldc = 4096;
+        gemm_bt<8, 1><<<dim3(32, 8, 6), blk, 0, stream>>>(agr);
+      }
+    } else {
+      int havePend = 0;
+      GA pendGA{};
+      for (int ci = 0, c0 = 0; c0 < NTOK; ++ci, c0 += CHKr) {
+        const int vc = (NTOK - c0 < CHKr) ? (NTOK - c0) : CHKr;
+        const int mt = cdiv(vc, 128);
+        const u16* kc = kb + (size_t)c0 * 1024;
+        u16* hhp = hhA[ci & 1];
+        u16* hTp = hTA[ci & 1];
+        if (vc < CHKr) hipMemsetAsync(hTp, 0, CB, stream);
+        {
+          GA agv{};
+          agv.A[0] = kc; agv.lda[0] = 1024;
+          agv.B[0] = Gt; agv.B[1] = Vt; agv.ldb[0] = 1024;
+          agv.C[0] = f1A[0]; agv.O1[0] = f2A[0]; agv.O1[1] = hhp; agv.OT[0] = hTp;
+          agv.M = vc; agv.N = 4096; agv.K = 1024; agv.ldc = 4096; agv.ldt = CHKr;
+          if (MODE == 1 && havePend) {
+            fused_gg<<<dim3(32, mt + 48, 1), blk, 0, stream>>>(pendGA, agv, mt);
+            havePend = 0;
+          } else {
+            gemm_gv<0><<<dim3(32, mt, 1), blk, 0, stream>>>(agv);
+          }
+        }
+        if (vc < CHKr) {
+          hipMemsetAsync(dzvT, 0, CB, stream);
+          hipMemsetAsync(dpTA[0], 0, DP, stream);
+        }
+        {
+          GA a = mk(Pt, hhp, dpTA[0], 1024, vc, 4096, 4096, 4096, CHKr);
+          a.OT[0] = dpBA[0]; a.ldt = 1024;
+          a.E0[0] = vT + c0; a.lde0 = NTOKA; a.p0 = inv2;
+          gemm64<2><<<dim3(cdiv(vc, 64), 16, 1), blk, 0, stream>>>(a);
+        }
+        if (vc < CHKr) hipMemsetAsync(hhp, 0, CB, stream);
+        {
+          GA a = mk(dpBA[0], Pb, hhp, vc, 4096, 1024, 1024, 1024, 0);
+          a.O1[0] = dzvT; a.ldt = CHKr;
+          a.E0[0] = f1A[0]; a.lde0 = 4096; a.E1[0] = f2A[0]; a.lde1 = 4096;
+          gemm_bt<5, 0><<<dim3(32, mt, 1), blk, 0, stream>>>(a);
+        }
+        {
+          GA a{};
+          a.A[0] = kT + c0; a.A[1] = kT + c0; a.A[2] = dpTA[0];
+          a.lda[0] = NTOKA; a.lda[1] = NTOKA; a.lda[2] = CHKr;
+          a.B[0] = hhp; a.B[1] = dzvT; a.B[2] = hTp;
+          a.ldb[0] = a.ldb[1] = a.ldb[2] = CHKr;
+          a.C[0] = gAll; a.C[1] = gAll + PM; a.C[2] = gAll + 2 * PM;
+          a.M = 1024; a.N = 4096; a.K = CHKr; a.ldc = 4096;
+          const int last = (c0 + CHKr >= NTOK);
+          if (MODE == 1 && !last) { pendGA = a; havePend = 1; }
+          else gemm_bt<8, 1><<<dim3(32, 8, 6), blk, 0, stream>>>(a);
+        }
       }
     }
     hipMemsetAsync(ssq, 0, 16, stream);
@@ -961,15 +1486,14 @@
     }
   }
 
-  gemm_bt<0, 0><<<dim3(32, 8, 1), blk, 0, stream>>>(
-      mk(projWt, Pb, PWt, 1024, 4096, 1024, 1024, 1024, 4096));
   {
-    GA a{};
-    a.A[0] = qb; a.lda[0] = 1024;
-    a.B[0] = Gt; a.B[1] = Vt; a.ldb[0] = 1024;
-    a.C[0] = hbuf;
-    a.M = NTOK; a.N = 4096; a.K = 1024; a.ldc = 4096;
-    gemm_gv<1><<<dim3(32, 86, 1), blk, 0, stream>>>(a);
+    GA agv{};
+    agv.A[0] = qb; agv.lda[0] = 1024;
+    agv.B[0] = Gt; agv.B[1] = Vt; agv.ldb[0] = 1024;
+    agv.C[0] = hbuf;
+    agv.M = NTOK; agv.N = 4096; agv.K = 1024; agv.ldc = 4096;
+    GA ap = mk(projWt, Pb, PWt, 1024, 4096, 1024, 1024, 1024, 4096);
+    fused_pg<<<dim3(32, 94, 1), blk, 0, stream>>>(ap, agv, 86);
   }
   {
     GA a = mk(hbuf, PWt, out, NTOK, 1024, 4096, 4096, 4096, 1024);
```
